# Performance work log

Measured on AMD Instinct MI355X. Metric: run time of the kernel, lower is better.

## Reference

```python
import jax, jax.numpy as jnp
import numpy as np

N_NODES = 4096
M_NODES = 8192
DIM = 256


def _symnorm(A):
    # D^{-1/2} A D^{-1/2} with eps, via row/col scaling (same math as diag matmuls)
    d = A.sum(axis=1) + 1e-5
    s = d ** -0.5
    return A * s[:, None] * s[None, :]


def _gat(A, X, W, a_src, a_dst, b):
    # Dense-form GATConv (PyG semantics): edges are nonzeros of A plus self loops.
    N = A.shape[0]
    H, F = a_src.shape
    Xp = (X @ W).reshape(N, H, F)                     # [N, H, F]
    src = jnp.einsum('nhf,hf->nh', Xp, a_src)         # score of source node j
    dst = jnp.einsum('nhf,hf->nh', Xp, a_dst)         # score of target node i
    logits = jax.nn.leaky_relu(dst[:, None, :] + src[None, :, :], negative_slope=0.2)  # [i, j, h]
    mask = (A != 0.0) | jnp.eye(N, dtype=bool)        # add_self_loops=True
    logits = jnp.where(mask[:, :, None], logits, -jnp.inf)
    alpha = jax.nn.softmax(logits, axis=1)            # softmax over neighbors j
    out = jnp.einsum('ijh,jhf->ihf', alpha, Xp).reshape(N, H * F) + b
    return out


def setup_inputs() -> dict:
    key = jax.random.key(0)
    ks = jax.random.split(key, 32)

    def p(i, shape, scale=0.05):
        return jax.random.normal(ks[i], shape, dtype=jnp.float32) * scale

    R = jax.random.normal(ks[0], (N_NODES, N_NODES), dtype=jnp.float32)
    A = jax.nn.relu((R + R.T) * 0.5)
    X = jax.random.normal(ks[1], (N_NODES, DIM), dtype=jnp.float32)
    return dict(
        A=A, X=X,
        # down GT0: GATConv(256, 128, heads=4) -> 512
        Wd0=p(2, (256, 512)), asd0=p(3, (4, 128)), add0=p(4, (4, 128)), bd0=p(5, (512,)),
        # down GT1: GATConv(512, 256, heads=4) -> 1024
        Wd1=p(6, (512, 1024)), asd1=p(7, (4, 256)), add1=p(8, (4, 256)), bd1=p(9, (1024,)),
        # pool projections (Linear(in, 1))
        wp0=p(10, (1, 512)), bp0=p(11, (1,)),
        wp1=p(12, (1, 1024)), bp1=p(13, (1,)),
        # bottom GT: GATConv(1024, 512, heads=2) -> 1024
        Wb=p(14, (1024, 1024)), asb=p(15, (2, 512)), adb=p(16, (2, 512)), bb=p(17, (1024,)),
        # up GT (reversed[0]): GATConv(1024, 128, heads=4) -> 512
        Wu0=p(18, (1024, 512)), asu0=p(19, (4, 128)), adu0=p(20, (4, 128)), bu0=p(21, (512,)),
        # up GT (reversed[1]): GATConv(512, 64, heads=4) -> 256
        Wu1=p(22, (512, 256)), asu1=p(23, (4, 64)), adu1=p(24, (4, 64)), bu1=p(25, (256,)),
        # upsampler Linear(n_nodes, m_nodes)
        Wup=p(26, (M_NODES, N_NODES)), bup=p(27, (M_NODES,)),
    )


def reference(A, X, Wd0, asd0, add0, bd0, Wd1, asd1, add1, bd1, wp0, bp0, wp1, bp1,
              Wb, asb, adb, bb, Wu0, asu0, adu0, bu0, Wu1, asu1, adu1, bu1, Wup, bup):
    N0 = A.shape[0]
    A0 = A + jnp.eye(N0, dtype=A.dtype)  # A_ = A + I (used throughout; normalized A is dead code)

    # ---- down level 0 ----
    X0 = jax.nn.relu(_gat(A0, X, Wd0, asd0, add0, bd0))            # [4096, 512]
    s0 = jax.nn.sigmoid(X0 @ wp0[0] + bp0[0])
    k0 = max(2, N0 // 2)                                            # int(0.5 * N)
    v0, idx0 = jax.lax.top_k(s0, k0)
    A1 = _symnorm(A0[idx0][:, idx0])                                # [2048, 2048]
    X1in = X0[idx0] * v0[:, None]

    # ---- down level 1 ----
    X1 = jax.nn.relu(_gat(A1, X1in, Wd1, asd1, add1, bd1))          # [2048, 1024]
    s1 = jax.nn.sigmoid(X1 @ wp1[0] + bp1[0])
    k1 = max(2, k0 // 2)
    v1, idx1 = jax.lax.top_k(s1, k1)
    A2 = _symnorm(A1[idx1][:, idx1])                                # [1024, 1024]
    X2in = X1[idx1] * v1[:, None]

    # ---- bottom ----
    Xb = jax.nn.relu(_gat(A2, X2in, Wb, asb, adb, bb))              # [1024, 1024]

    # ---- up level 0: unpool to level-1 graph ----
    h = jnp.zeros((k0, Xb.shape[1]), Xb.dtype).at[idx1].set(Xb)
    Xu0 = jax.nn.relu(_gat(A1, h, Wu0, asu0, adu0, bu0))            # [2048, 512]
    rec0 = jax.nn.relu(Xu0 @ Xu0.T)

    # ---- up level 1: unpool to original graph ----
    h = jnp.zeros((N0, Xu0.shape[1]), Xu0.dtype).at[idx0].set(Xu0)
    Xu1 = jax.nn.relu(_gat(A0, h, Wu1, asu1, adu1, bu1))            # [4096, 256]
    rec1 = jax.nn.relu(Xu1 @ Xu1.T)

    # ---- upsampler: Linear over node dim, softmax over feature dim, reconstruct adjacency ----
    Z = jax.nn.softmax(Wup @ Xu1 + bup[:, None], axis=1)            # [8192, 256]
    A_up = jax.nn.relu(Z @ Z.T)                                     # [8192, 8192]
    return (A_up, A0, A1, rec0, rec1)
```

## Files before the change

kernel.cpp:

```cpp
#include <hip/hip_runtime.h>
#include <math.h>


typedef short bf16x8 __attribute__((ext_vector_type(8)));
typedef float f32x4 __attribute__((ext_vector_type(4)));

static __device__ __forceinline__ float wave_sum64(float v) {
#pragma unroll
  for (int off = 32; off; off >>= 1) v += __shfl_down(v, off);
  return v;
}

static __device__ __forceinline__ unsigned short f2b(float x) {
  unsigned u = __float_as_uint(x);
  unsigned r = (u + 0x7fffu + ((u >> 16) & 1u)) >> 16;
  return (unsigned short)r;
}

static __device__ __forceinline__ float b2f(unsigned short h) {
  return __uint_as_float(((unsigned)h) << 16);
}

__global__ void k_add_eye(const float* __restrict__ A, float* __restrict__ O) {
  size_t i = ((size_t)blockIdx.x * 256 + threadIdx.x) * 4;
  size_t r = i >> 12, c = i & 4095;
  float4 v = *reinterpret_cast<const float4*>(&A[i]);
  if (r >= c && r < c + 4) ((float*)&v)[r - c] += 1.f;
  *reinterpret_cast<float4*>(&O[i]) = v;
}

__global__ void k_fill0(float* __restrict__ p, int n) {
  int stride = gridDim.x * 256;
  for (int i = blockIdx.x * 256 + threadIdx.x; i < n; i += stride) p[i] = 0.f;
}

__global__ void k_scatter_ones(const int* __restrict__ idx, float* __restrict__ m, int k) {
  int i = blockIdx.x * 256 + threadIdx.x;
  if (i < k) m[idx[i]] = 1.f;
}

__global__ void k_f32_to_bf16(const float* __restrict__ S, unsigned short* __restrict__ D,
                              int n) {
  int stride = gridDim.x * 1024;
  for (int i = (blockIdx.x * 256 + threadIdx.x) * 4; i < n; i += stride) {
    float4 v = *reinterpret_cast<const float4*>(&S[i]);
    uint2 o;
    o.x = (unsigned)f2b(v.x) | ((unsigned)f2b(v.y) << 16);
    o.y = (unsigned)f2b(v.z) | ((unsigned)f2b(v.w) << 16);
    *reinterpret_cast<uint2*>(&D[i]) = o;
  }
}

__global__ void k_split3(const float* __restrict__ S, unsigned short* __restrict__ D,
                         size_t PS, int n) {
  int stride = gridDim.x * 1024;
  for (int i = (blockIdx.x * 256 + threadIdx.x) * 4; i < n; i += stride) {
    float4 v = *reinterpret_cast<const float4*>(&S[i]);
    float xv[4] = {v.x, v.y, v.z, v.w};
    unsigned short o1[4], o2[4], o3[4];
#pragma unroll
    for (int e = 0; e < 4; ++e) {
      float x = xv[e];
      unsigned short a = f2b(x);
      float r1 = x - b2f(a);
      unsigned short b = f2b(r1);
      float r2 = r1 - b2f(b);
      o1[e] = a; o2[e] = b; o3[e] = f2b(r2);
    }
    *reinterpret_cast<uint2*>(&D[i]) = *reinterpret_cast<const uint2*>(o1);
    *reinterpret_cast<uint2*>(&D[PS + i]) = *reinterpret_cast<const uint2*>(o2);
    *reinterpret_cast<uint2*>(&D[2 * PS + i]) = *reinterpret_cast<const uint2*>(o3);
  }
}

__global__ __launch_bounds__(256) void k_transpose_bf16(const float* __restrict__ S, int ldS,
    unsigned short* __restrict__ D, int R, int Cc) {
  __shared__ unsigned short T[64][72];
  int r0 = blockIdx.y << 6, c0 = blockIdx.x << 6;
  int tid = threadIdx.x;
  int tr = tid >> 4, tc4 = (tid & 15) << 2;
#pragma unroll
  for (int q = 0; q < 4; ++q) {
    int row = tr + q * 16;
    float4 v = *reinterpret_cast<const float4*>(&S[(size_t)(r0 + row) * ldS + c0 + tc4]);
    T[tc4 + 0][row] = f2b(v.x);
    T[tc4 + 1][row] = f2b(v.y);
    T[tc4 + 2][row] = f2b(v.z);
    T[tc4 + 3][row] = f2b(v.w);
  }
  __syncthreads();
#pragma unroll
  for (int q = 0; q < 4; ++q) {
    int row = tr + q * 16;
    *reinterpret_cast<uint2*>(&D[(size_t)(c0 + row) * R + r0 + tc4]) =
        *reinterpret_cast<const uint2*>(&T[row][tc4]);
  }
}

__global__ __launch_bounds__(256) void k_transpose_bf16h(const float* __restrict__ S, int ldS,
    int F, unsigned short* __restrict__ D, int R) {
  __shared__ unsigned short T[64][72];
  int h = blockIdx.z;
  int r0 = blockIdx.y << 6, c0 = blockIdx.x << 6;
  int tid = threadIdx.x;
  int tr = tid >> 4, tc4 = (tid & 15) << 2;
#pragma unroll
  for (int q = 0; q < 4; ++q) {
    int row = tr + q * 16;
    float4 v = *reinterpret_cast<const float4*>(&S[(size_t)(r0 + row) * ldS + h * F + c0 + tc4]);
    T[tc4 + 0][row] = f2b(v.x);
    T[tc4 + 1][row] = f2b(v.y);
    T[tc4 + 2][row] = f2b(v.z);
    T[tc4 + 3][row] = f2b(v.w);
  }
  __syncthreads();
#pragma unroll
  for (int q = 0; q < 4; ++q) {
    int row = tr + q * 16;
    *reinterpret_cast<uint2*>(&D[((size_t)h * F + c0 + row) * R + r0 + tc4]) =
        *reinterpret_cast<const uint2*>(&T[row][tc4]);
  }
}

__global__ __launch_bounds__(256) void k_transpose_split(const float* __restrict__ S, int ldS,
    int F, unsigned short* __restrict__ D, int R, size_t PS) {
  __shared__ unsigned short T[3][64][72];
  int h = blockIdx.z;
  int c0 = blockIdx.x << 6, r0 = blockIdx.y << 6;
  int tid = threadIdx.x;
  int tr = tid >> 4, tc4 = (tid & 15) << 2;
#pragma unroll
  for (int q = 0; q < 4; ++q) {
    int row = tr + q * 16;
    float4 v = *reinterpret_cast<const float4*>(&S[(size_t)(r0 + row) * ldS + h * F + c0 + tc4]);
    float xv[4] = {v.x, v.y, v.z, v.w};
#pragma unroll
    for (int e = 0; e < 4; ++e) {
      float x = xv[e];
      unsigned short h1 = f2b(x);
      float r1 = x - b2f(h1);
      unsigned short h2 = f2b(r1);
      float r2 = r1 - b2f(h2);
      T[0][tc4 + e][row] = h1;
      T[1][tc4 + e][row] = h2;
      T[2][tc4 + e][row] = f2b(r2);
    }
  }
  __syncthreads();
#pragma unroll
  for (int p = 0; p < 3; ++p)
#pragma unroll
    for (int q = 0; q < 4; ++q) {
      int row = tr + q * 16;
      *reinterpret_cast<uint2*>(&D[p * PS + (size_t)(h * F + c0 + row) * R + r0 + tc4]) =
          *reinterpret_cast<const uint2*>(&T[p][row][tc4]);
    }
}

__global__ __launch_bounds__(256, 2) void k_gemm_x6_bt(const unsigned short* __restrict__ As,
    size_t APS, const unsigned short* __restrict__ BTs, size_t BPS, float* __restrict__ C,
    int M, int N, int K) {
  __shared__ __align__(16) unsigned short Ai[3][128 * 40];
  __shared__ __align__(16) unsigned short Bj[3][128 * 40];
  int tid = threadIdx.x;
  int m0 = blockIdx.y << 7, n0 = blockIdx.x << 7;
  int lane = tid & 63, w = tid >> 6;
  int lr = lane & 15, kb = lane >> 4;
  int wr = (w >> 1) << 6, wc = (w & 1) << 6;
  int sr = tid >> 1, sc = (tid & 1) << 4;
  f32x4 acc[4][4] = {};
  for (int k0 = 0; k0 < K; k0 += 32) {
    __syncthreads();
#pragma unroll
    for (int p = 0; p < 3; ++p) {
      const unsigned short* ga = &As[p * APS + (size_t)(m0 + sr) * K + k0 + sc];
      *reinterpret_cast<uint4*>(&Ai[p][sr * 40 + sc]) = *reinterpret_cast<const uint4*>(ga);
      *reinterpret_cast<uint4*>(&Ai[p][sr * 40 + sc + 8]) =
          *reinterpret_cast<const uint4*>(ga + 8);
      const unsigned short* gb = &BTs[p * BPS + (size_t)(n0 + sr) * K + k0 + sc];
      *reinterpret_cast<uint4*>(&Bj[p][sr * 40 + sc]) = *reinterpret_cast<const uint4*>(gb);
      *reinterpret_cast<uint4*>(&Bj[p][sr * 40 + sc + 8]) =
          *reinterpret_cast<const uint4*>(gb + 8);
    }
    __syncthreads();
    bf16x8 af[4][3], bf_[4][3];
#pragma unroll
    for (int m = 0; m < 4; ++m)
#pragma unroll
      for (int p = 0; p < 3; ++p)
        af[m][p] = *reinterpret_cast<const bf16x8*>(&Ai[p][(wr + m * 16 + lr) * 40 + kb * 8]);
#pragma unroll
    for (int n = 0; n < 4; ++n)
#pragma unroll
      for (int p = 0; p < 3; ++p)
        bf_[n][p] = *reinterpret_cast<const bf16x8*>(&Bj[p][(wc + n * 16 + lr) * 40 + kb * 8]);
#pragma unroll
    for (int m = 0; m < 4; ++m)
#pragma unroll
      for (int n = 0; n < 4; ++n) {
        acc[m][n] = __builtin_amdgcn_mfma_f32_16x16x32_bf16(af[m][0], bf_[n][0], acc[m][n], 0, 0, 0);
        acc[m][n] = __builtin_amdgcn_mfma_f32_16x16x32_bf16(af[m][0], bf_[n][1], acc[m][n], 0, 0, 0);
        acc[m][n] = __builtin_amdgcn_mfma_f32_16x16x32_bf16(af[m][1], bf_[n][0], acc[m][n], 0, 0, 0);
        acc[m][n] = __builtin_amdgcn_mfma_f32_16x16x32_bf16(af[m][0], bf_[n][2], acc[m][n], 0, 0, 0);
        acc[m][n] = __builtin_amdgcn_mfma_f32_16x16x32_bf16(af[m][2], bf_[n][0], acc[m][n], 0, 0, 0);
        acc[m][n] = __builtin_amdgcn_mfma_f32_16x16x32_bf16(af[m][1], bf_[n][1], acc[m][n], 0, 0, 0);
      }
  }
  int orow = m0 + wr + (lane >> 4) * 4;
  int ocol = n0 + wc + lr;
#pragma unroll
  for (int m = 0; m < 4; ++m)
#pragma unroll
    for (int n = 0; n < 4; ++n)
#pragma unroll
      for (int r = 0; r < 4; ++r)
        C[(size_t)(orow + m * 16 + r) * N + ocol + n * 16] = acc[m][n][r];
}

__global__ __launch_bounds__(512) void k_gat_x6(const float* __restrict__ Adj, int N,
    const unsigned short* __restrict__ XpS, size_t PS,
    const float* __restrict__ src, const float* __restrict__ dst,
    float* __restrict__ P, float* __restrict__ dP, int HF, int F, int jchunk) {
  __shared__ __align__(16) unsigned short wB[2][3][128 * 40];
  __shared__ __align__(16) unsigned short xB[2][3][128 * 40];
  int ftiles = F >> 7;
  int h = blockIdx.x / ftiles;
  int ft = blockIdx.x % ftiles;
  int f0 = ft << 7;
  int H = HF / F;
  int i0 = blockIdx.y << 7;
  int jb0 = blockIdx.z * jchunk;
  int tid = threadIdx.x;
  bool producer = tid < 256;
  int ntiles = jchunk >> 5;

  int sj4 = (tid & 7) << 2, si = tid >> 3;
  int xf = tid >> 1, xj8 = (tid & 1) << 3;
  float di[4];
  float dsum[4] = {0.f, 0.f, 0.f, 0.f};
  const unsigned short* xg = XpS + ((size_t)h * F + f0 + (producer ? xf : 0)) * N;
  float4 aw[4];
  float s4[4];
  uint4 xv[3][2];

  auto load_tile = [&](int jb) {
#pragma unroll
    for (int e = 0; e < 4; ++e) s4[e] = src[(jb + sj4 + e) * H + h];
#pragma unroll
    for (int q = 0; q < 4; ++q)
      aw[q] = *reinterpret_cast<const float4*>(&Adj[(size_t)(i0 + si + q * 32) * N + jb + sj4]);
#pragma unroll
    for (int p = 0; p < 3; ++p) {
      xv[p][0] = *reinterpret_cast<const uint4*>(&xg[p * PS + jb + xj8]);
      xv[p][1] = *reinterpret_cast<const uint4*>(&xg[p * PS + jb + xj8 + 16]);
    }
  };
  auto emit_tile = [&](int b, int jb) {
#pragma unroll
    for (int q = 0; q < 4; ++q) {
      int gi = i0 + si + q * 32;
      float dq = di[q];
      const float* a = (const float*)&aw[q];
      unsigned short h1[4], h2[4], h3[4];
      float ds = 0.f;
#pragma unroll
      for (int e = 0; e < 4; ++e) {
        float wv = 0.f;
        if (a[e] != 0.f || (jb + sj4 + e) == gi) {
          float tt = dq + s4[e];
          tt = tt >= 0.f ? tt : 0.2f * tt;
          wv = __expf(tt);
        }
        ds += wv;
        unsigned u1 = __float_as_uint(wv);
        h1[e] = (unsigned short)(u1 >> 16);
        float r1 = wv - __uint_as_float(u1 & 0xffff0000u);
        unsigned u2 = __float_as_uint(r1);
        h2[e] = (unsigned short)(u2 >> 16);
        float r2 = r1 - __uint_as_float(u2 & 0xffff0000u);
        h3[e] = (unsigned short)(__float_as_uint(r2) >> 16);
      }
      dsum[q] += ds;
      int ro = (si + q * 32) * 40 + sj4;
      uint2 o;
      o.x = (unsigned)h1[0] | ((unsigned)h1[1] << 16);
      o.y = (unsigned)h1[2] | ((unsigned)h1[3] << 16);
      *reinterpret_cast<uint2*>(&wB[b][0][ro]) = o;
      o.x = (unsigned)h2[0] | ((unsigned)h2[1] << 16);
      o.y = (unsigned)h2[2] | ((unsigned)h2[3] << 16);
      *reinterpret_cast<uint2*>(&wB[b][1][ro]) = o;
      o.x = (unsigned)h3[0] | ((unsigned)h3[1] << 16);
      o.y = (unsigned)h3[2] | ((unsigned)h3[3] << 16);
      *reinterpret_cast<uint2*>(&wB[b][2][ro]) = o;
    }
#pragma unroll
    for (int p = 0; p < 3; ++p) {
      *reinterpret_cast<uint4*>(&xB[b][p][xf * 40 + xj8]) = xv[p][0];
      *reinterpret_cast<uint4*>(&xB[b][p][xf * 40 + xj8 + 16]) = xv[p][1];
    }
  };

  int lane = tid & 63, cw = (tid >> 6) - 4;
  int clr = lane & 15, ckb = lane >> 4;
  int wr = ((cw >> 1) & 1) << 6, wf = (cw & 1) << 6;
  f32x4 acc[4][4] = {};

  if (producer) {
#pragma unroll
    for (int q = 0; q < 4; ++q) di[q] = dst[(i0 + si + q * 32) * H + h];
    load_tile(jb0);
    emit_tile(0, jb0);
    if (ntiles > 1) load_tile(jb0 + 32);
  }
  __syncthreads();
  for (int t = 0; t < ntiles; ++t) {
    if (producer) {
      int tn = t + 1;
      if (tn < ntiles) {
        emit_tile(tn & 1, jb0 + tn * 32);
        if (tn + 1 < ntiles) load_tile(jb0 + (tn + 1) * 32);
      }
    } else {
      int b = t & 1;
      bf16x8 af[4][3], bf_[4][3];
#pragma unroll
      for (int m = 0; m < 4; ++m)
#pragma unroll
        for (int p = 0; p < 3; ++p)
          af[m][p] =
              *reinterpret_cast<const bf16x8*>(&wB[b][p][(wr + m * 16 + clr) * 40 + ckb * 8]);
#pragma unroll
      for (int n = 0; n < 4; ++n)
#pragma unroll
        for (int p = 0; p < 3; ++p)
          bf_[n][p] =
              *reinterpret_cast<const bf16x8*>(&xB[b][p][(wf + n * 16 + clr) * 40 + ckb * 8]);
#pragma unroll
      for (int m = 0; m < 4; ++m)
#pragma unroll
        for (int n = 0; n < 4; ++n) {
          acc[m][n] = __builtin_amdgcn_mfma_f32_16x16x32_bf16(af[m][0], bf_[n][0], acc[m][n], 0, 0, 0);
          acc[m][n] = __builtin_amdgcn_mfma_f32_16x16x32_bf16(af[m][0], bf_[n][1], acc[m][n], 0, 0, 0);
          acc[m][n] = __builtin_amdgcn_mfma_f32_16x16x32_bf16(af[m][1], bf_[n][0], acc[m][n], 0, 0, 0);
          acc[m][n] = __builtin_amdgcn_mfma_f32_16x16x32_bf16(af[m][0], bf_[n][2], acc[m][n], 0, 0, 0);
          acc[m][n] = __builtin_amdgcn_mfma_f32_16x16x32_bf16(af[m][2], bf_[n][0], acc[m][n], 0, 0, 0);
          acc[m][n] = __builtin_amdgcn_mfma_f32_16x16x32_bf16(af[m][1], bf_[n][1], acc[m][n], 0, 0, 0);
        }
    }
    __syncthreads();
  }
  if (producer) {
    if (ft == 0) {
#pragma unroll
      for (int q = 0; q < 4; ++q) {
        float v = dsum[q];
        v += __shfl_xor(v, 1);
        v += __shfl_xor(v, 2);
        v += __shfl_xor(v, 4);
        if ((tid & 7) == 0)
          dP[(size_t)blockIdx.z * N * H + (i0 + si + q * 32) * H + h] = v;
      }
    }
  } else {
    float* Pc = P + (size_t)blockIdx.z * N * HF;
    int orow = i0 + wr + (lane >> 4) * 4;
    int ocol = h * F + f0 + wf + clr;
#pragma unroll
    for (int m = 0; m < 4; ++m)
#pragma unroll
      for (int n = 0; n < 4; ++n)
#pragma unroll
        for (int r = 0; r < 4; ++r)
          Pc[(size_t)(orow + m * 16 + r) * HF + ocol + n * 16] = acc[m][n][r];
  }
}

__global__ __launch_bounds__(256) void k_gat_mfma(const float* __restrict__ Adj, int N,
    const unsigned short* __restrict__ XpT,
    const float* __restrict__ src, const float* __restrict__ dst,
    float* __restrict__ P, float* __restrict__ dP, int HF, int F, int jchunk) {
  __shared__ __align__(16) unsigned short wL[256][40];
  __shared__ __align__(16) unsigned short xT[64][40];
  __shared__ float dsl[256];
  int ftiles = F >> 6;
  int h = blockIdx.x / ftiles;
  int ft = blockIdx.x % ftiles;
  int f0 = ft << 6;
  int H = HF / F;
  int i0 = blockIdx.y << 8;
  int jb0 = blockIdx.z * jchunk;
  int tid = threadIdx.x;
  int lane = tid & 63, w = tid >> 6;
  int lr = lane & 15, kb = lane >> 4;
  dsl[tid] = dst[(i0 + tid) * H + h];
  int sj4 = (tid & 7) << 2;
  int si = tid >> 3;
  int xf = tid >> 2;
  int xj8 = (tid & 3) << 3;
  const unsigned short* xg = XpT + ((size_t)h * F + f0 + xf) * N;
  float dsum[8] = {};
  f32x4 acc[4][4] = {};
  for (int jb = jb0; jb < jb0 + jchunk; jb += 32) {
    __syncthreads();
    float s4[4];
#pragma unroll
    for (int e = 0; e < 4; ++e) s4[e] = src[(jb + sj4 + e) * H + h];
#pragma unroll
    for (int q = 0; q < 8; ++q) {
      int i = si + q * 32;
      int gi = i0 + i;
      float4 av = *reinterpret_cast<const float4*>(&Adj[(size_t)gi * N + jb + sj4]);
      float di = dsl[i];
      float vv[4] = {av.x, av.y, av.z, av.w};
      unsigned short wb[4];
      float ds = 0.f;
#pragma unroll
      for (int e = 0; e < 4; ++e) {
        float wv = 0.f;
        if (vv[e] != 0.f || (jb + sj4 + e) == gi) {
          float t = di + s4[e];
          t = t >= 0.f ? t : 0.2f * t;
          wv = __expf(t);
        }
        ds += wv;
        wb[e] = f2b(wv);
      }
      dsum[q] += ds;
      *reinterpret_cast<uint2*>(&wL[i][sj4]) = *reinterpret_cast<const uint2*>(wb);
    }
    *reinterpret_cast<uint4*>(&xT[xf][xj8]) = *reinterpret_cast<const uint4*>(&xg[jb + xj8]);
    __syncthreads();
    bf16x8 a[4], b[4];
#pragma unroll
    for (int m = 0; m < 4; ++m)
      a[m] = *reinterpret_cast<const bf16x8*>(&wL[w * 64 + m * 16 + lr][kb * 8]);
#pragma unroll
    for (int n = 0; n < 4; ++n)
      b[n] = *reinterpret_cast<const bf16x8*>(&xT[n * 16 + lr][kb * 8]);
#pragma unroll
    for (int m = 0; m < 4; ++m)
#pragma unroll
      for (int n = 0; n < 4; ++n)
        acc[m][n] = __builtin_amdgcn_mfma_f32_16x16x32_bf16(a[m], b[n], acc[m][n], 0, 0, 0);
  }
  if (ft == 0) {
#pragma unroll
    for (int q = 0; q < 8; ++q) {
      float v = dsum[q];
      v += __shfl_xor(v, 1);
      v += __shfl_xor(v, 2);
      v += __shfl_xor(v, 4);
      if ((tid & 7) == 0)
        dP[(size_t)blockIdx.z * N * H + (i0 + si + q * 32) * H + h] = v;
    }
  }
  float* Pc = P + (size_t)blockIdx.z * N * HF;
  int orow = i0 + w * 64 + (lane >> 4) * 4;
  int ocol = h * F + f0 + (lane & 15);
#pragma unroll
  for (int m = 0; m < 4; ++m)
#pragma unroll
    for (int n = 0; n < 4; ++n)
#pragma unroll
      for (int r = 0; r < 4; ++r)
        Pc[(size_t)(orow + m * 16 + r) * HF + ocol + n * 16] = acc[m][n][r];
}

__global__ void k_gat_reduce(const float* __restrict__ P, int nch, size_t chstride,
    const float* __restrict__ dP, size_t dstride, const float* __restrict__ bias,
    float* __restrict__ Out, int HF, int F, int n_total) {
  int e = (blockIdx.x * 256 + threadIdx.x) * 4;
  if (e >= n_total) return;
  float4 s = *reinterpret_cast<const float4*>(&P[e]);
  for (int c = 1; c < nch; ++c) {
    float4 v = *reinterpret_cast<const float4*>(&P[c * chstride + e]);
    s.x += v.x; s.y += v.y; s.z += v.z; s.w += v.w;
  }
  int i = e / HF;
  int hf = e - i * HF;
  int h = hf / F;
  float den = 0.f;
  for (int c = 0; c < nch; ++c) den += dP[c * dstride + i * (HF / F) + h];
  float inv = 1.f / den;
  float4 bz = *reinterpret_cast<const float4*>(&bias[hf]);
  float4 o;
  o.x = fmaxf(fmaf(s.x, inv, bz.x), 0.f);
  o.y = fmaxf(fmaf(s.y, inv, bz.y), 0.f);
  o.z = fmaxf(fmaf(s.z, inv, bz.z), 0.f);
  o.w = fmaxf(fmaf(s.w, inv, bz.w), 0.f);
  *reinterpret_cast<float4*>(&Out[e]) = o;
}

__global__ __launch_bounds__(256) void k_syrk_mfma(const unsigned short* __restrict__ G,
    int M, int Kd, float* __restrict__ C) {
  if (blockIdx.x < blockIdx.y) return;
  __shared__ __align__(16) unsigned short Ai[128 * 40];
  __shared__ __align__(16) unsigned short Bj[128 * 40];
  int tid = threadIdx.x;
  int i0 = blockIdx.y << 7, j0 = blockIdx.x << 7;
  int srow = tid >> 1, scol = (tid & 1) << 3;
  int lane = tid & 63, w = tid >> 6;
  int wr = (w >> 1) << 6, wc = (w & 1) << 6;
  int lr = lane & 15, kb = lane >> 4;
  f32x4 acc[4][4] = {};
  const unsigned short* gA = G + (size_t)i0 * Kd;
  const unsigned short* gB = G + (size_t)j0 * Kd;
  for (int k0 = 0; k0 < Kd; k0 += 32) {
    __syncthreads();
#pragma unroll
    for (int kk = 0; kk < 32; kk += 16) {
      *reinterpret_cast<uint4*>(&Ai[srow * 40 + scol + kk]) =
          *reinterpret_cast<const uint4*>(&gA[(size_t)srow * Kd + k0 + scol + kk]);
      *reinterpret_cast<uint4*>(&Bj[srow * 40 + scol + kk]) =
          *reinterpret_cast<const uint4*>(&gB[(size_t)srow * Kd + k0 + scol + kk]);
    }
    __syncthreads();
    bf16x8 a[4], b[4];
#pragma unroll
    for (int m = 0; m < 4; ++m)
      a[m] = *reinterpret_cast<const bf16x8*>(&Ai[(wr + m * 16 + lr) * 40 + kb * 8]);
#pragma unroll
    for (int n = 0; n < 4; ++n)
      b[n] = *reinterpret_cast<const bf16x8*>(&Bj[(wc + n * 16 + lr) * 40 + kb * 8]);
#pragma unroll
    for (int m = 0; m < 4; ++m)
#pragma unroll
      for (int n = 0; n < 4; ++n)
        acc[m][n] = __builtin_amdgcn_mfma_f32_16x16x32_bf16(a[m], b[n], acc[m][n], 0, 0, 0);
  }
  int orow = i0 + wr + (lane >> 4) * 4;
  int ocol = j0 + wc + (lane & 15);
  bool mirror = (j0 != i0);
#pragma unroll
  for (int m = 0; m < 4; ++m)
#pragma unroll
    for (int n = 0; n < 4; ++n) {
      float4 v;
      v.x = fmaxf(acc[m][n][0], 0.f);
      v.y = fmaxf(acc[m][n][1], 0.f);
      v.z = fmaxf(acc[m][n][2], 0.f);
      v.w = fmaxf(acc[m][n][3], 0.f);
#pragma unroll
      for (int r = 0; r < 4; ++r)
        C[(size_t)(orow + m * 16 + r) * M + ocol + n * 16] = ((const float*)&v)[r];
      if (mirror)
        *reinterpret_cast<float4*>(
            &C[(size_t)(j0 + wc + n * 16 + lr) * M + i0 + wr + m * 16 + (lane >> 4) * 4]) = v;
    }
}

__global__ __launch_bounds__(256) void k_gemm_mfma_bt(const unsigned short* __restrict__ Amat,
    const unsigned short* __restrict__ BT, const float* __restrict__ bias,
    float* __restrict__ C, int M, int N, int Kd) {
  __shared__ __align__(16) unsigned short Ai[128 * 40];
  __shared__ __align__(16) unsigned short Bj[128 * 40];
  int tid = threadIdx.x;
  int m0 = blockIdx.y << 7, n0 = blockIdx.x << 7;
  int srow = tid >> 1, scol = (tid & 1) << 3;
  int lane = tid & 63, w = tid >> 6;
  int wr = (w >> 1) << 6, wc = (w & 1) << 6;
  int lr = lane & 15, kb = lane >> 4;
  f32x4 acc[4][4] = {};
  const unsigned short* gA = Amat + (size_t)m0 * Kd;
  const unsigned short* gB = BT + (size_t)n0 * Kd;
  for (int k0 = 0; k0 < Kd; k0 += 32) {
    __syncthreads();
#pragma unroll
    for (int kk = 0; kk < 32; kk += 16) {
      *reinterpret_cast<uint4*>(&Ai[srow * 40 + scol + kk]) =
          *reinterpret_cast<const uint4*>(&gA[(size_t)srow * Kd + k0 + scol + kk]);
      *reinterpret_cast<uint4*>(&Bj[srow * 40 + scol + kk]) =
          *reinterpret_cast<const uint4*>(&gB[(size_t)srow * Kd + k0 + scol + kk]);
    }
    __syncthreads();
    bf16x8 a[4], b[4];
#pragma unroll
    for (int m = 0; m < 4; ++m)
      a[m] = *reinterpret_cast<const bf16x8*>(&Ai[(wr + m * 16 + lr) * 40 + kb * 8]);
#pragma unroll
    for (int n = 0; n < 4; ++n)
      b[n] = *reinterpret_cast<const bf16x8*>(&Bj[(wc + n * 16 + lr) * 40 + kb * 8]);
#pragma unroll
    for (int m = 0; m < 4; ++m)
#pragma unroll
      for (int n = 0; n < 4; ++n)
        acc[m][n] = __builtin_amdgcn_mfma_f32_16x16x32_bf16(a[m], b[n], acc[m][n], 0, 0, 0);
  }
  int orow = m0 + wr + (lane >> 4) * 4;
  int ocol = n0 + wc + (lane & 15);
#pragma unroll
  for (int m = 0; m < 4; ++m)
#pragma unroll
    for (int n = 0; n < 4; ++n)
#pragma unroll
      for (int r = 0; r < 4; ++r) {
        float rb = bias ? bias[orow + m * 16 + r] : 0.f;
        C[(size_t)(orow + m * 16 + r) * N + ocol + n * 16] = acc[m][n][r] + rb;
      }
}

__global__ __launch_bounds__(512) void k_gemm_aup(const float* __restrict__ Wg,
    const unsigned short* __restrict__ BT, float* __restrict__ Pz, int Mtot, int Ktot,
    int kc_len) {
  __shared__ __align__(16) unsigned short Ai[128 * 40];
  __shared__ __align__(16) unsigned short Bj[256 * 40];
  int tid = threadIdx.x;
  int m0 = blockIdx.y << 7;
  int k0base = blockIdx.x * kc_len;
  int lane = tid & 63, w = tid >> 6;
  int wr = (w >> 2) << 6, wc = (w & 3) << 6;
  int lr = lane & 15, kb = lane >> 4;
  int ar = tid >> 2, ac8 = (tid & 3) << 3;
  int br = tid >> 1, bc16 = (tid & 1) << 4;
  f32x4 acc[4][4] = {};
  for (int kk = 0; kk < kc_len; kk += 32) {
    int k0 = k0base + kk;
    __syncthreads();
    {
      const float* arow = &Wg[(size_t)(m0 + ar) * Ktot + k0 + ac8];
      float4 v0 = *reinterpret_cast<const float4*>(arow);
      float4 v1 = *reinterpret_cast<const float4*>(arow + 4);
      unsigned short t8[8] = {f2b(v0.x), f2b(v0.y), f2b(v0.z), f2b(v0.w),
                              f2b(v1.x), f2b(v1.y), f2b(v1.z), f2b(v1.w)};
      *reinterpret_cast<uint4*>(&Ai[ar * 40 + ac8]) = *reinterpret_cast<const uint4*>(t8);
      const unsigned short* brow = &BT[(size_t)br * Ktot + k0 + bc16];
      *reinterpret_cast<uint4*>(&Bj[br * 40 + bc16]) = *reinterpret_cast<const uint4*>(brow);
      *reinterpret_cast<uint4*>(&Bj[br * 40 + bc16 + 8]) =
          *reinterpret_cast<const uint4*>(brow + 8);
    }
    __syncthreads();
    bf16x8 a[4], b[4];
#pragma unroll
    for (int m = 0; m < 4; ++m)
      a[m] = *reinterpret_cast<const bf16x8*>(&Ai[(wr + m * 16 + lr) * 40 + kb * 8]);
#pragma unroll
    for (int n = 0; n < 4; ++n)
      b[n] = *reinterpret_cast<const bf16x8*>(&Bj[(wc + n * 16 + lr) * 40 + kb * 8]);
#pragma unroll
    for (int m = 0; m < 4; ++m)
#pragma unroll
      for (int n = 0; n < 4; ++n)
        acc[m][n] = __builtin_amdgcn_mfma_f32_16x16x32_bf16(a[m], b[n], acc[m][n], 0, 0, 0);
  }
  float* outp = Pz + (size_t)blockIdx.x * Mtot * 256;
  int orow = m0 + wr + (lane >> 4) * 4;
  int ocol = wc + (lane & 15);
#pragma unroll
  for (int m = 0; m < 4; ++m)
#pragma unroll
    for (int n = 0; n < 4; ++n)
#pragma unroll
      for (int r = 0; r < 4; ++r)
        outp[(size_t)(orow + m * 16 + r) * 256 + ocol + n * 16] = acc[m][n][r];
}

__global__ __launch_bounds__(256) void k_softmax_fuse(const float* __restrict__ Pz, int nch,
    size_t chstride, const float* __restrict__ bias, unsigned short* __restrict__ ZB) {
  int row = blockIdx.x, tid = threadIdx.x;
  size_t e = (size_t)row * 256 + tid;
  float x = bias[row];
  for (int c = 0; c < nch; ++c) x += Pz[c * chstride + e];
  float m = x;
#pragma unroll
  for (int off = 32; off; off >>= 1) m = fmaxf(m, __shfl_down(m, off));
  __shared__ float red[4];
  __shared__ float bm, bs;
  if ((tid & 63) == 0) red[tid >> 6] = m;
  __syncthreads();
  if (tid == 0) bm = fmaxf(fmaxf(red[0], red[1]), fmaxf(red[2], red[3]));
  __syncthreads();
  float ev = expf(x - bm);
  float sm = wave_sum64(ev);
  __syncthreads();
  if ((tid & 63) == 0) red[tid >> 6] = sm;
  __syncthreads();
  if (tid == 0) bs = red[0] + red[1] + red[2] + red[3];
  __syncthreads();
  ZB[e] = f2b(ev / bs);
}

__global__ void k_src_dst(const float* __restrict__ Xp, const float* __restrict__ a_src,
    const float* __restrict__ a_dst, float* __restrict__ src, float* __restrict__ dst,
    int H, int F) {
  int n = blockIdx.x;
  int h = threadIdx.x >> 6, lane = threadIdx.x & 63;
  const float* x = Xp + ((size_t)n * H + h) * F;
  const float* as = a_src + h * F;
  const float* ad = a_dst + h * F;
  float ps = 0.f, pd = 0.f;
  for (int f = lane; f < F; f += 64) {
    float xv = x[f];
    ps = fmaf(xv, as[f], ps);
    pd = fmaf(xv, ad[f], pd);
  }
  ps = wave_sum64(ps);
  pd = wave_sum64(pd);
  if (lane == 0) { src[n * H + h] = ps; dst[n * H + h] = pd; }
}

__global__ __launch_bounds__(256) void k_score(const float* __restrict__ Xf,
    const float* __restrict__ wv, const float* __restrict__ bsc, float* __restrict__ s, int D) {
  int row = blockIdx.x * 4 + (threadIdx.x >> 6);
  int lane = threadIdx.x & 63;
  const float* x = Xf + (size_t)row * D;
  float p = 0.f;
  for (int f = lane; f < D; f += 64) p = fmaf(x[f], wv[f], p);
  p = wave_sum64(p);
  if (lane == 0) s[row] = 1.f / (1.f + expf(-(p + bsc[0])));
}

__global__ __launch_bounds__(256) void k_topk_rank(const float* __restrict__ s, int n, int k,
    int* __restrict__ idx, float* __restrict__ vals) {
  extern __shared__ unsigned long long keys[];
  int tid = threadIdx.x;
  for (int j = tid; j < n; j += 256) {
    unsigned u = __float_as_uint(s[j]);
    unsigned ord = (u & 0x80000000u) ? ~u : (u | 0x80000000u);
    keys[j] = ((unsigned long long)ord << 32) | (unsigned)(~j);
  }
  __syncthreads();
  int i = blockIdx.x * 256 + tid;
  unsigned long long mykey = keys[i];
  int rank = 0;
#pragma unroll 4
  for (int j = 0; j < n; ++j) rank += (keys[j] > mykey);
  if (rank < k) { idx[rank] = i; vals[rank] = s[i]; }
}

__global__ __launch_bounds__(256) void k_rowsum_mask(const float* __restrict__ A0, int N,
    const int* __restrict__ idx, const float* __restrict__ m, float* __restrict__ sv) {
  int i = blockIdx.x, tid = threadIdx.x;
  const float* row = A0 + (size_t)idx[i] * N;
  float p = 0.f;
  for (int j = tid * 4; j < N; j += 1024) {
    float4 a = *reinterpret_cast<const float4*>(&row[j]);
    float4 b = *reinterpret_cast<const float4*>(&m[j]);
    p += a.x * b.x + a.y * b.y + a.z * b.z + a.w * b.w;
  }
  p = wave_sum64(p);
  __shared__ float red[4];
  if ((tid & 63) == 0) red[tid >> 6] = p;
  __syncthreads();
  if (tid == 0) sv[i] = rsqrtf(red[0] + red[1] + red[2] + red[3] + 1e-5f);
}

__global__ __launch_bounds__(256) void k_gatherT(const float* __restrict__ A0, int N,
    const int* __restrict__ idx, float* __restrict__ T1, int k) {
  __shared__ float T[64][65];
  int i0 = blockIdx.x << 6, c0 = blockIdx.y << 6;
  int tid = threadIdx.x;
  int tr = tid >> 4, tc4 = (tid & 15) << 2;
#pragma unroll
  for (int q = 0; q < 4; ++q) {
    int row = tr + q * 16;
    float4 v = *reinterpret_cast<const float4*>(&A0[(size_t)idx[i0 + row] * N + c0 + tc4]);
    T[tc4 + 0][row] = v.x; T[tc4 + 1][row] = v.y; T[tc4 + 2][row] = v.z; T[tc4 + 3][row] = v.w;
  }
  __syncthreads();
#pragma unroll
  for (int q = 0; q < 4; ++q) {
    int row = tr + q * 16;
    float4 o;
    o.x = T[row][tc4]; o.y = T[row][tc4 + 1]; o.z = T[row][tc4 + 2]; o.w = T[row][tc4 + 3];
    *reinterpret_cast<float4*>(&T1[(size_t)(c0 + row) * k + i0 + tc4]) = o;
  }
}

__global__ void k_scaleT(const float* __restrict__ T1, int k, const int* __restrict__ idx,
    const float* __restrict__ sv, float* __restrict__ A1) {
  int j = blockIdx.y;
  int i = (blockIdx.x * 256 + threadIdx.x) * 4;
  float sj = sv[j];
  const float* r = T1 + (size_t)idx[j] * k;
  float4 v = *reinterpret_cast<const float4*>(&r[i]);
  float4 s = *reinterpret_cast<const float4*>(&sv[i]);
  v.x *= sj * s.x; v.y *= sj * s.y; v.z *= sj * s.z; v.w *= sj * s.w;
  *reinterpret_cast<float4*>(&A1[(size_t)j * k + i]) = v;
}

__global__ void k_gather_mat(const float* __restrict__ Asrc, int lda,
    const int* __restrict__ idx, float* __restrict__ B, int k) {
  int j = blockIdx.x * 256 + threadIdx.x;
  int i = blockIdx.y;
  B[(size_t)i * k + j] = Asrc[(size_t)idx[i] * lda + idx[j]];
}

__global__ void k_gather_scale_rows(const float* __restrict__ Xs, int D,
    const int* __restrict__ idx, const float* __restrict__ v, float* __restrict__ Xo) {
  int f = blockIdx.x * 256 + threadIdx.x;
  int i = blockIdx.y;
  Xo[(size_t)i * D + f] = Xs[(size_t)idx[i] * D + f] * v[i];
}

__global__ void k_scatter_rows(const float* __restrict__ P, int D, const int* __restrict__ idx,
                               float* __restrict__ Xo) {
  int f = blockIdx.x * 256 + threadIdx.x;
  int i = blockIdx.y;
  Xo[(size_t)idx[i] * D + f] = P[(size_t)i * D + f];
}

extern "C" void kernel_launch(void* const* d_in, const int* in_sizes, int n_in,
                              void* d_out, int out_size, void* d_ws, size_t ws_size,
                              hipStream_t stream) {
  const float* A    = (const float*)d_in[0];
  const float* X    = (const float*)d_in[1];
  const float* Wd0  = (const float*)d_in[2];
  const float* asd0 = (const float*)d_in[3];
  const float* add0 = (const float*)d_in[4];
  const float* bd0  = (const float*)d_in[5];
  const float* Wd1  = (const float*)d_in[6];
  const float* asd1 = (const float*)d_in[7];
  const float* add1 = (const float*)d_in[8];
  const float* bd1  = (const float*)d_in[9];
  const float* wp0  = (const float*)d_in[10];
  const float* bp0  = (const float*)d_in[11];
  const float* wp1  = (const float*)d_in[12];
  const float* bp1  = (const float*)d_in[13];
  const float* Wb   = (const float*)d_in[14];
  const float* asb  = (const float*)d_in[15];
  const float* adb  = (const float*)d_in[16];
  const float* bb   = (const float*)d_in[17];
  const float* Wu0  = (const float*)d_in[18];
  const float* asu0 = (const float*)d_in[19];
  const float* adu0 = (const float*)d_in[20];
  const float* bu0  = (const float*)d_in[21];
  const float* Wu1  = (const float*)d_in[22];
  const float* asu1 = (const float*)d_in[23];
  const float* adu1 = (const float*)d_in[24];
  const float* bu1  = (const float*)d_in[25];
  const float* Wup  = (const float*)d_in[26];
  const float* bup  = (const float*)d_in[27];
  (void)in_sizes; (void)n_in; (void)out_size; (void)ws_size;

  float* out  = (float*)d_out;
  float* Aup  = out;
  float* A0   = out + 67108864ULL;
  float* A1   = A0 + 16777216ULL;
  float* rec0 = A1 + 4194304ULL;
  float* rec1 = rec0 + 4194304ULL;

  float* S = Aup;
  size_t off = 0;
  auto nxt = [&](size_t n) { float* p = S + off; off += (n + 1023) & ~(size_t)1023; return p; };
  float* Xp0  = nxt(4096 * 512);
  float* X0   = nxt(4096 * 512);
  float* src0 = nxt(4096 * 4);
  float* dst0 = nxt(4096 * 4);
  float* sc0  = nxt(4096);
  int*   idx0 = (int*)nxt(2048);
  float* v0   = nxt(2048);
  float* sv0  = nxt(2048);
  float* maskv = nxt(4096);
  float* X1in = nxt(2048 * 512);
  float* Xp1  = nxt(2048 * 1024);
  float* X1   = nxt(2048 * 1024);
  float* src1 = nxt(2048 * 4);
  float* dst1 = nxt(2048 * 4);
  float* sc1  = nxt(2048);
  int*   idx1 = (int*)nxt(1024);
  float* v1   = nxt(1024);
  float* A2m  = nxt(1024 * 1024);
  float* X2in = nxt(1024 * 1024);
  float* Xpb  = nxt(1024 * 1024);
  float* Xb   = nxt(1024 * 1024);
  float* srcb = nxt(1024 * 2);
  float* dstb = nxt(1024 * 2);
  float* Pu0  = nxt(1024 * 512);
  float* Xpu0 = nxt(2048 * 512);
  float* Xu0  = nxt(2048 * 512);
  float* su0  = nxt(2048 * 4);
  float* du0  = nxt(2048 * 4);
  float* Pu1  = nxt(2048 * 256);
  float* Xpu1 = nxt(4096 * 256);
  float* su1  = nxt(4096 * 4);
  float* du1  = nxt(4096 * 4);
  float* dPp  = nxt(8 * 4096 * 4);
  float* P    = nxt((size_t)8 * 4096 * 512);
  float* T1   = nxt((size_t)4096 * 2048);
  unsigned short* XpS  = (unsigned short*)nxt(3200000);
  unsigned short* XSp  = (unsigned short*)nxt(1572864);
  unsigned short* Wd0T = (unsigned short*)nxt(196608);
  unsigned short* Wd1T = (unsigned short*)nxt(786432);
  unsigned short* XpT  = (unsigned short*)nxt(524288);
  unsigned short* X2inB = (unsigned short*)nxt(524288);
  unsigned short* XbB   = (unsigned short*)nxt(524288);
  unsigned short* WbT   = (unsigned short*)nxt(524288);
  unsigned short* Wu0T  = (unsigned short*)nxt(262144);
  unsigned short* Wu1T  = (unsigned short*)nxt(65536);

  float* W = (float*)d_ws;
  float* Xu1 = W;
  unsigned short* Xu1B = (unsigned short*)(W + 1048576);
  unsigned short* Xu0B = (unsigned short*)(W + 1048576 + 524288);

  float* Pz = rec1;
  unsigned short* ZB = (unsigned short*)(rec1 + 4 * 2097152);
  unsigned short* Xu1T = (unsigned short*)(rec1 + 4 * 2097152 + 1048576);

  const size_t PS0 = (size_t)4 * 128 * 4096;
  const size_t PS1 = (size_t)4 * 256 * 2048;

  k_add_eye<<<16384, 256, 0, stream>>>(A, A0);

  k_split3<<<1024, 256, 0, stream>>>(X, XSp, (size_t)4096 * 256, 4096 * 256);
  k_transpose_split<<<dim3(8, 4, 1), 256, 0, stream>>>(Wd0, 512, 512, Wd0T, 256,
                                                       (size_t)512 * 256);
  k_gemm_x6_bt<<<dim3(4, 32), 256, 0, stream>>>(XSp, (size_t)4096 * 256, Wd0T,
                                                (size_t)512 * 256, Xp0, 4096, 512, 256);
  k_src_dst<<<4096, 256, 0, stream>>>(Xp0, asd0, add0, src0, dst0, 4, 128);
  k_transpose_split<<<dim3(2, 64, 4), 256, 0, stream>>>(Xp0, 512, 128, XpS, 4096, PS0);
  k_gat_x6<<<dim3(4, 32, 2), 512, 0, stream>>>(A0, 4096, XpS, PS0, src0, dst0, P, dPp, 512,
                                               128, 2048);
  k_gat_reduce<<<2048, 256, 0, stream>>>(P, 2, (size_t)4096 * 512, dPp, (size_t)4096 * 4, bd0,
                                         X0, 512, 128, 4096 * 512);
  k_score<<<1024, 256, 0, stream>>>(X0, wp0, bp0, sc0, 512);
  k_topk_rank<<<16, 256, 4096 * 8, stream>>>(sc0, 4096, 2048, idx0, v0);
  k_fill0<<<16, 256, 0, stream>>>(maskv, 4096);
  k_scatter_ones<<<8, 256, 0, stream>>>(idx0, maskv, 2048);
  k_rowsum_mask<<<2048, 256, 0, stream>>>(A0, 4096, idx0, maskv, sv0);
  k_gatherT<<<dim3(32, 64), 256, 0, stream>>>(A0, 4096, idx0, T1, 2048);
  k_scaleT<<<dim3(2, 2048), 256, 0, stream>>>(T1, 2048, idx0, sv0, A1);
  k_gather_scale_rows<<<dim3(2, 2048), 256, 0, stream>>>(X0, 512, idx0, v0, X1in);

  k_split3<<<1024, 256, 0, stream>>>(X1in, XSp, (size_t)2048 * 512, 2048 * 512);
  k_transpose_split<<<dim3(16, 8, 1), 256, 0, stream>>>(Wd1, 1024, 1024, Wd1T, 512,
                                                        (size_t)1024 * 512);
  k_gemm_x6_bt<<<dim3(8, 16), 256, 0, stream>>>(XSp, (size_t)2048 * 512, Wd1T,
                                                (size_t)1024 * 512, Xp1, 2048, 1024, 512);
  k_src_dst<<<2048, 256, 0, stream>>>(Xp1, asd1, add1, src1, dst1, 4, 256);
  k_transpose_split<<<dim3(4, 32, 4), 256, 0, stream>>>(Xp1, 1024, 256, XpS, 2048, PS1);
  k_gat_x6<<<dim3(8, 16, 2), 512, 0, stream>>>(A1, 2048, XpS, PS1, src1, dst1, P, dPp, 1024,
                                               256, 1024);
  k_gat_reduce<<<2048, 256, 0, stream>>>(P, 2, (size_t)2048 * 1024, dPp, (size_t)2048 * 4, bd1,
                                         X1, 1024, 256, 2048 * 1024);
  k_score<<<512, 256, 0, stream>>>(X1, wp1, bp1, sc1, 1024);
  k_topk_rank<<<8, 256, 2048 * 8, stream>>>(sc1, 2048, 1024, idx1, v1);
  k_gather_mat<<<dim3(4, 1024), 256, 0, stream>>>(A1, 2048, idx1, A2m, 1024);
  k_gather_scale_rows<<<dim3(4, 1024), 256, 0, stream>>>(X1, 1024, idx1, v1, X2in);

  k_f32_to_bf16<<<1024, 256, 0, stream>>>(X2in, X2inB, 1024 * 1024);
  k_transpose_bf16<<<dim3(16, 16), 256, 0, stream>>>(Wb, 1024, WbT, 1024, 1024);
  k_gemm_mfma_bt<<<dim3(8, 8), 256, 0, stream>>>(X2inB, WbT, nullptr, Xpb, 1024, 1024, 1024);
  k_src_dst<<<1024, 128, 0, stream>>>(Xpb, asb, adb, srcb, dstb, 2, 512);
  k_transpose_bf16h<<<dim3(8, 16, 2), 256, 0, stream>>>(Xpb, 1024, 512, XpT, 1024);
  k_gat_mfma<<<dim3(16, 4, 8), 256, 0, stream>>>(A2m, 1024, XpT, srcb, dstb, P, dPp, 1024, 512,
                                                 128);
  k_gat_reduce<<<1024, 256, 0, stream>>>(P, 8, (size_t)1024 * 1024, dPp, (size_t)1024 * 2, bb,
                                         Xb, 1024, 512, 1024 * 1024);

  k_f32_to_bf16<<<1024, 256, 0, stream>>>(Xb, XbB, 1024 * 1024);
  k_transpose_bf16<<<dim3(8, 16), 256, 0, stream>>>(Wu0, 512, Wu0T, 1024, 512);
  k_gemm_mfma_bt<<<dim3(4, 8), 256, 0, stream>>>(XbB, Wu0T, nullptr, Pu0, 1024, 512, 1024);
  k_fill0<<<1024, 256, 0, stream>>>(Xpu0, 2048 * 512);
  k_scatter_rows<<<dim3(2, 1024), 256, 0, stream>>>(Pu0, 512, idx1, Xpu0);
  k_src_dst<<<2048, 256, 0, stream>>>(Xpu0, asu0, adu0, su0, du0, 4, 128);
  k_transpose_bf16h<<<dim3(2, 32, 4), 256, 0, stream>>>(Xpu0, 512, 128, XpT, 2048);
  k_gat_mfma<<<dim3(8, 8, 8), 256, 0, stream>>>(A1, 2048, XpT, su0, du0, P, dPp, 512, 128, 256);
  k_gat_reduce<<<1024, 256, 0, stream>>>(P, 8, (size_t)2048 * 512, dPp, (size_t)2048 * 4, bu0,
                                         Xu0, 512, 128, 2048 * 512);
  k_f32_to_bf16<<<1024, 256, 0, stream>>>(Xu0, Xu0B, 2048 * 512);

  k_transpose_bf16<<<dim3(4, 8), 256, 0, stream>>>(Wu1, 256, Wu1T, 512, 256);
  k_gemm_mfma_bt<<<dim3(2, 16), 256, 0, stream>>>(Xu0B, Wu1T, nullptr, Pu1, 2048, 256, 512);
  k_fill0<<<1024, 256, 0, stream>>>(Xpu1, 4096 * 256);
  k_scatter_rows<<<dim3(1, 2048), 256, 0, stream>>>(Pu1, 256, idx0, Xpu1);
  k_src_dst<<<4096, 256, 0, stream>>>(Xpu1, asu1, adu1, su1, du1, 4, 64);
  k_transpose_bf16h<<<dim3(1, 64, 4), 256, 0, stream>>>(Xpu1, 256, 64, XpT, 4096);
  k_gat_mfma<<<dim3(4, 16, 8), 256, 0, stream>>>(A0, 4096, XpT, su1, du1, P, dPp, 256, 64, 512);
  k_gat_reduce<<<1024, 256, 0, stream>>>(P, 8, (size_t)4096 * 256, dPp, (size_t)4096 * 4, bu1,
                                         Xu1, 256, 64, 4096 * 256);
  k_f32_to_bf16<<<1024, 256, 0, stream>>>(Xu1, Xu1B, 4096 * 256);
  k_transpose_bf16<<<dim3(4, 64), 256, 0, stream>>>(Xu1, 256, Xu1T, 4096, 256);

  k_gemm_aup<<<dim3(4, 64), 512, 0, stream>>>(Wup, Xu1T, Pz, 8192, 4096, 1024);
  k_softmax_fuse<<<8192, 256, 0, stream>>>(Pz, 4, (size_t)8192 * 256, bup, ZB);
  k_syrk_mfma<<<dim3(64, 64), 256, 0, stream>>>(ZB, 8192, 256, Aup);

  k_syrk_mfma<<<dim3(32, 32), 256, 0, stream>>>(Xu1B, 4096, 256, rec1);
  k_syrk_mfma<<<dim3(16, 16), 256, 0, stream>>>(Xu0B, 2048, 512, rec0);
}
```

Measured before the change: 1.144 ms.

## Restructure GAT kernels, fuse gather/scale/convert steps, and emit bf16 from reduce

Replaces the producer/consumer k_gat_x6 with a simpler single-buffer kernel that uses all eight waves for both weight generation and MFMA, and splits the j range four ways. k_gat_mfma becomes a templated k_gat_b16 that handles several heads per block with 128-row tiles. Gather+scale+split/convert is fused into one kernel, the mask scatter is folded into top-k, and the reduce writes bf16 directly, which removes the separate f32-to-bf16 passes and fp32 intermediates. This cuts launches and memory traffic. The cost is more partial-sum traffic from the extra j splits, and the GAT kernel loses its overlap of loads with compute.

```diff
diff --git a/kernel.cpp b/kernel.cpp
--- a/kernel.cpp
+++ b/kernel.cpp
@@ -32,23 +32,6 @@
 __global__ void k_fill0(float* __restrict__ p, int n) {
   int stride = gridDim.x * 256;
   for (int i = blockIdx.x * 256 + threadIdx.x; i < n; i += stride) p[i] = 0.f;
-}
-
-__global__ void k_scatter_ones(const int* __restrict__ idx, float* __restrict__ m, int k) {
-  int i = blockIdx.x * 256 + threadIdx.x;
-  if (i < k) m[idx[i]] = 1.f;
-}
-
-__global__ void k_f32_to_bf16(const float* __restrict__ S, unsigned short* __restrict__ D,
-                              int n) {
-  int stride = gridDim.x * 1024;
-  for (int i = (blockIdx.x * 256 + threadIdx.x) * 4; i < n; i += stride) {
-    float4 v = *reinterpret_cast<const float4*>(&S[i]);
-    uint2 o;
-    o.x = (unsigned)f2b(v.x) | ((unsigned)f2b(v.y) << 16);
-    o.y = (unsigned)f2b(v.z) | ((unsigned)f2b(v.w) << 16);
-    *reinterpret_cast<uint2*>(&D[i]) = o;
-  }
 }
 
 __global__ void k_split3(const float* __restrict__ S, unsigned short* __restrict__ D,
@@ -73,6 +56,43 @@
   }
 }
 
+__global__ void k_gather_scale_split3(const float* __restrict__ Xs, int Dd,
+    const int* __restrict__ idx, const float* __restrict__ v,
+    unsigned short* __restrict__ D, size_t PS) {
+  int i = blockIdx.y;
+  int f = (blockIdx.x * 256 + threadIdx.x) * 4;
+  if (f >= Dd) return;
+  float vi = v[i];
+  float4 x4 = *reinterpret_cast<const float4*>(&Xs[(size_t)idx[i] * Dd + f]);
+  float xv[4] = {x4.x * vi, x4.y * vi, x4.z * vi, x4.w * vi};
+  unsigned short o1[4], o2[4], o3[4];
+#pragma unroll
+  for (int e = 0; e < 4; ++e) {
+    float x = xv[e];
+    unsigned short a = f2b(x);
+    float r1 = x - b2f(a);
+    unsigned short b = f2b(r1);
+    float r2 = r1 - b2f(b);
+    o1[e] = a; o2[e] = b; o3[e] = f2b(r2);
+  }
+  size_t e0 = (size_t)i * Dd + f;
+  *reinterpret_cast<uint2*>(&D[e0]) = *reinterpret_cast<const uint2*>(o1);
+  *reinterpret_cast<uint2*>(&D[PS + e0]) = *reinterpret_cast<const uint2*>(o2);
+  *reinterpret_cast<uint2*>(&D[2 * PS + e0]) = *reinterpret_cast<const uint2*>(o3);
+}
+
+__global__ void k_gather_scale_b16(const float* __restrict__ Xs, int Dd,
+    const int* __restrict__ idx, const float* __restrict__ v,
+    unsigned short* __restrict__ D) {
+  int i = blockIdx.y;
+  int f = (blockIdx.x * 256 + threadIdx.x) * 4;
+  if (f >= Dd) return;
+  float vi = v[i];
+  float4 x4 = *reinterpret_cast<const float4*>(&Xs[(size_t)idx[i] * Dd + f]);
+  unsigned short o[4] = {f2b(x4.x * vi), f2b(x4.y * vi), f2b(x4.z * vi), f2b(x4.w * vi)};
+  *reinterpret_cast<uint2*>(&D[(size_t)i * Dd + f]) = *reinterpret_cast<const uint2*>(o);
+}
+
 __global__ __launch_bounds__(256) void k_transpose_bf16(const float* __restrict__ S, int ldS,
     unsigned short* __restrict__ D, int R, int Cc) {
   __shared__ unsigned short T[64][72];
@@ -87,6 +107,29 @@
     T[tc4 + 1][row] = f2b(v.y);
     T[tc4 + 2][row] = f2b(v.z);
     T[tc4 + 3][row] = f2b(v.w);
+  }
+  __syncthreads();
+#pragma unroll
+  for (int q = 0; q < 4; ++q) {
+    int row = tr + q * 16;
+    *reinterpret_cast<uint2*>(&D[(size_t)(c0 + row) * R + r0 + tc4]) =
+        *reinterpret_cast<const uint2*>(&T[row][tc4]);
+  }
+}
+
+__global__ __launch_bounds__(256) void k_transpose_bb(const unsigned short* __restrict__ S,
+    int ldS, unsigned short* __restrict__ D, int R, int Cc) {
+  __shared__ unsigned short T[64][72];
+  int r0 = blockIdx.y << 6, c0 = blockIdx.x << 6;
+  int tid = threadIdx.x;
+  int tr = tid >> 4, tc4 = (tid & 15) << 2;
+#pragma unroll
+  for (int q = 0; q < 4; ++q) {
+    int row = tr + q * 16;
+    uint2 v = *reinterpret_cast<const uint2*>(&S[(size_t)(r0 + row) * ldS + c0 + tc4]);
+    const unsigned short* p = (const unsigned short*)&v;
+    T[tc4 + 0][row] = p[0]; T[tc4 + 1][row] = p[1];
+    T[tc4 + 2][row] = p[2]; T[tc4 + 3][row] = p[3];
   }
   __syncthreads();
 #pragma unroll
@@ -217,57 +260,57 @@
         C[(size_t)(orow + m * 16 + r) * N + ocol + n * 16] = acc[m][n][r];
 }
 
-__global__ __launch_bounds__(512) void k_gat_x6(const float* __restrict__ Adj, int N,
+__global__ __launch_bounds__(512, 4) void k_gat_x6(const float* __restrict__ Adj, int N,
     const unsigned short* __restrict__ XpS, size_t PS,
     const float* __restrict__ src, const float* __restrict__ dst,
-    float* __restrict__ P, float* __restrict__ dP, int HF, int F, int jchunk) {
-  __shared__ __align__(16) unsigned short wB[2][3][128 * 40];
-  __shared__ __align__(16) unsigned short xB[2][3][128 * 40];
-  int ftiles = F >> 7;
-  int h = blockIdx.x / ftiles;
-  int ft = blockIdx.x % ftiles;
-  int f0 = ft << 7;
-  int H = HF / F;
+    float* __restrict__ P, float* __restrict__ dP, int HF, int Ffull, int FP, int jchunk) {
+  __shared__ __align__(16) unsigned short wL[3][128 * 40];
+  __shared__ __align__(16) unsigned short xL[3][128 * 40];
+  __shared__ float dstL[128];
+  __shared__ float srcL[32];
+  int H = HF / Ffull;
+  int h = blockIdx.x / FP;
+  int fp = blockIdx.x % FP;
+  int f0 = fp << 7;
   int i0 = blockIdx.y << 7;
   int jb0 = blockIdx.z * jchunk;
   int tid = threadIdx.x;
-  bool producer = tid < 256;
+  int si = tid >> 2, sj8 = (tid & 3) << 3;
+  int lane = tid & 63, w = tid >> 6;
+  int lr = lane & 15, kb = lane >> 4;
+  int fs = w << 4;
+  if (tid < 128) dstL[tid] = dst[(i0 + tid) * H + h];
+  float dsum = 0.f;
+  f32x4 acc[8] = {};
   int ntiles = jchunk >> 5;
-
-  int sj4 = (tid & 7) << 2, si = tid >> 3;
-  int xf = tid >> 1, xj8 = (tid & 1) << 3;
-  float di[4];
-  float dsum[4] = {0.f, 0.f, 0.f, 0.f};
-  const unsigned short* xg = XpS + ((size_t)h * F + f0 + (producer ? xf : 0)) * N;
-  float4 aw[4];
-  float s4[4];
-  uint4 xv[3][2];
-
-  auto load_tile = [&](int jb) {
-#pragma unroll
-    for (int e = 0; e < 4; ++e) s4[e] = src[(jb + sj4 + e) * H + h];
-#pragma unroll
-    for (int q = 0; q < 4; ++q)
-      aw[q] = *reinterpret_cast<const float4*>(&Adj[(size_t)(i0 + si + q * 32) * N + jb + sj4]);
-#pragma unroll
-    for (int p = 0; p < 3; ++p) {
-      xv[p][0] = *reinterpret_cast<const uint4*>(&xg[p * PS + jb + xj8]);
-      xv[p][1] = *reinterpret_cast<const uint4*>(&xg[p * PS + jb + xj8 + 16]);
-    }
-  };
-  auto emit_tile = [&](int b, int jb) {
-#pragma unroll
-    for (int q = 0; q < 4; ++q) {
-      int gi = i0 + si + q * 32;
-      float dq = di[q];
-      const float* a = (const float*)&aw[q];
-      unsigned short h1[4], h2[4], h3[4];
+  const unsigned short* xbase = XpS + ((size_t)h * Ffull + f0) * N;
+  for (int t = 0; t < ntiles; ++t) {
+    int jb = jb0 + (t << 5);
+    __syncthreads();
+    if (tid < 32) srcL[tid] = src[(jb + tid) * H + h];
+    {
+      int frow = tid >> 2;
+#pragma unroll
+      for (int p = 0; p < 3; ++p)
+        *reinterpret_cast<uint4*>(&xL[p][frow * 40 + sj8]) =
+            *reinterpret_cast<const uint4*>(&xbase[p * PS + (size_t)frow * N + jb + sj8]);
+    }
+    float4 av0 = *reinterpret_cast<const float4*>(&Adj[(size_t)(i0 + si) * N + jb + sj8]);
+    float4 av1 = *reinterpret_cast<const float4*>(&Adj[(size_t)(i0 + si) * N + jb + sj8 + 4]);
+    __syncthreads();
+    {
+      int gi = i0 + si;
+      float dq = dstL[si];
+      const float* a0 = (const float*)&av0;
+      const float* a1 = (const float*)&av1;
+      unsigned short h1[8], h2[8], h3[8];
       float ds = 0.f;
 #pragma unroll
-      for (int e = 0; e < 4; ++e) {
+      for (int e = 0; e < 8; ++e) {
+        float a = e < 4 ? a0[e] : a1[e - 4];
         float wv = 0.f;
-        if (a[e] != 0.f || (jb + sj4 + e) == gi) {
-          float tt = dq + s4[e];
+        if (a != 0.f || (jb + sj8 + e) == gi) {
+          float tt = dq + srcL[sj8 + e];
           tt = tt >= 0.f ? tt : 0.2f * tt;
           wv = __expf(tt);
         }
@@ -280,195 +323,148 @@
         float r2 = r1 - __uint_as_float(u2 & 0xffff0000u);
         h3[e] = (unsigned short)(__float_as_uint(r2) >> 16);
       }
-      dsum[q] += ds;
-      int ro = (si + q * 32) * 40 + sj4;
-      uint2 o;
-      o.x = (unsigned)h1[0] | ((unsigned)h1[1] << 16);
-      o.y = (unsigned)h1[2] | ((unsigned)h1[3] << 16);
-      *reinterpret_cast<uint2*>(&wB[b][0][ro]) = o;
-      o.x = (unsigned)h2[0] | ((unsigned)h2[1] << 16);
-      o.y = (unsigned)h2[2] | ((unsigned)h2[3] << 16);
-      *reinterpret_cast<uint2*>(&wB[b][1][ro]) = o;
-      o.x = (unsigned)h3[0] | ((unsigned)h3[1] << 16);
-      o.y = (unsigned)h3[2] | ((unsigned)h3[3] << 16);
-      *reinterpret_cast<uint2*>(&wB[b][2][ro]) = o;
-    }
-#pragma unroll
-    for (int p = 0; p < 3; ++p) {
-      *reinterpret_cast<uint4*>(&xB[b][p][xf * 40 + xj8]) = xv[p][0];
-      *reinterpret_cast<uint4*>(&xB[b][p][xf * 40 + xj8 + 16]) = xv[p][1];
-    }
-  };
-
-  int lane = tid & 63, cw = (tid >> 6) - 4;
-  int clr = lane & 15, ckb = lane >> 4;
-  int wr = ((cw >> 1) & 1) << 6, wf = (cw & 1) << 6;
-  f32x4 acc[4][4] = {};
-
-  if (producer) {
-#pragma unroll
-    for (int q = 0; q < 4; ++q) di[q] = dst[(i0 + si + q * 32) * H + h];
-    load_tile(jb0);
-    emit_tile(0, jb0);
-    if (ntiles > 1) load_tile(jb0 + 32);
-  }
-  __syncthreads();
-  for (int t = 0; t < ntiles; ++t) {
-    if (producer) {
-      int tn = t + 1;
-      if (tn < ntiles) {
-        emit_tile(tn & 1, jb0 + tn * 32);
-        if (tn + 1 < ntiles) load_tile(jb0 + (tn + 1) * 32);
-      }
-    } else {
-      int b = t & 1;
-      bf16x8 af[4][3], bf_[4][3];
-#pragma unroll
-      for (int m = 0; m < 4; ++m)
-#pragma unroll
-        for (int p = 0; p < 3; ++p)
-          af[m][p] =
-              *reinterpret_cast<const bf16x8*>(&wB[b][p][(wr + m * 16 + clr) * 40 + ckb * 8]);
-#pragma unroll
-      for (int n = 0; n < 4; ++n)
-#pragma unroll
-        for (int p = 0; p < 3; ++p)
-          bf_[n][p] =
-              *reinterpret_cast<const bf16x8*>(&xB[b][p][(wf + n * 16 + clr) * 40 + ckb * 8]);
-#pragma unroll
-      for (int m = 0; m < 4; ++m)
-#pragma unroll
-        for (int n = 0; n < 4; ++n) {
-          acc[m][n] = __builtin_amdgcn_mfma_f32_16x16x32_bf16(af[m][0], bf_[n][0], acc[m][n], 0, 0, 0);
-          acc[m][n] = __builtin_amdgcn_mfma_f32_16x16x32_bf16(af[m][0], bf_[n][1], acc[m][n], 0, 0, 0);
-          acc[m][n] = __builtin_amdgcn_mfma_f32_16x16x32_bf16(af[m][1], bf_[n][0], acc[m][n], 0, 0, 0);
-          acc[m][n] = __builtin_amdgcn_mfma_f32_16x16x32_bf16(af[m][0], bf_[n][2], acc[m][n], 0, 0, 0);
-          acc[m][n] = __builtin_amdgcn_mfma_f32_16x16x32_bf16(af[m][2], bf_[n][0], acc[m][n], 0, 0, 0);
-          acc[m][n] = __builtin_amdgcn_mfma_f32_16x16x32_bf16(af[m][1], bf_[n][1], acc[m][n], 0, 0, 0);
-        }
-    }
-    __syncthreads();
-  }
-  if (producer) {
-    if (ft == 0) {
-#pragma unroll
-      for (int q = 0; q < 4; ++q) {
-        float v = dsum[q];
-        v += __shfl_xor(v, 1);
-        v += __shfl_xor(v, 2);
-        v += __shfl_xor(v, 4);
-        if ((tid & 7) == 0)
-          dP[(size_t)blockIdx.z * N * H + (i0 + si + q * 32) * H + h] = v;
-      }
-    }
-  } else {
-    float* Pc = P + (size_t)blockIdx.z * N * HF;
-    int orow = i0 + wr + (lane >> 4) * 4;
-    int ocol = h * F + f0 + wf + clr;
-#pragma unroll
-    for (int m = 0; m < 4; ++m)
-#pragma unroll
-      for (int n = 0; n < 4; ++n)
-#pragma unroll
-        for (int r = 0; r < 4; ++r)
-          Pc[(size_t)(orow + m * 16 + r) * HF + ocol + n * 16] = acc[m][n][r];
-  }
-}
-
-__global__ __launch_bounds__(256) void k_gat_mfma(const float* __restrict__ Adj, int N,
+      dsum += ds;
+      *reinterpret_cast<uint4*>(&wL[0][si * 40 + sj8]) = *reinterpret_cast<const uint4*>(h1);
+      *reinterpret_cast<uint4*>(&wL[1][si * 40 + sj8]) = *reinterpret_cast<const uint4*>(h2);
+      *reinterpret_cast<uint4*>(&wL[2][si * 40 + sj8]) = *reinterpret_cast<const uint4*>(h3);
+    }
+    __syncthreads();
+    bf16x8 bf_[3];
+#pragma unroll
+    for (int p = 0; p < 3; ++p)
+      bf_[p] = *reinterpret_cast<const bf16x8*>(&xL[p][(fs + lr) * 40 + kb * 8]);
+#pragma unroll
+    for (int m = 0; m < 8; ++m) {
+      bf16x8 af[3];
+#pragma unroll
+      for (int p = 0; p < 3; ++p)
+        af[p] = *reinterpret_cast<const bf16x8*>(&wL[p][(m * 16 + lr) * 40 + kb * 8]);
+      acc[m] = __builtin_amdgcn_mfma_f32_16x16x32_bf16(af[0], bf_[0], acc[m], 0, 0, 0);
+      acc[m] = __builtin_amdgcn_mfma_f32_16x16x32_bf16(af[0], bf_[1], acc[m], 0, 0, 0);
+      acc[m] = __builtin_amdgcn_mfma_f32_16x16x32_bf16(af[1], bf_[0], acc[m], 0, 0, 0);
+      acc[m] = __builtin_amdgcn_mfma_f32_16x16x32_bf16(af[0], bf_[2], acc[m], 0, 0, 0);
+      acc[m] = __builtin_amdgcn_mfma_f32_16x16x32_bf16(af[2], bf_[0], acc[m], 0, 0, 0);
+      acc[m] = __builtin_amdgcn_mfma_f32_16x16x32_bf16(af[1], bf_[1], acc[m], 0, 0, 0);
+    }
+  }
+  if (fp == 0) {
+    float v = dsum;
+    v += __shfl_xor(v, 1);
+    v += __shfl_xor(v, 2);
+    if ((tid & 3) == 0)
+      dP[(size_t)blockIdx.z * N * H + (i0 + si) * H + h] = v;
+  }
+  float* Pc = P + (size_t)blockIdx.z * N * HF;
+  int orow = i0 + (lane >> 4) * 4;
+  int ocol = h * Ffull + f0 + fs + lr;
+#pragma unroll
+  for (int m = 0; m < 8; ++m)
+#pragma unroll
+    for (int r = 0; r < 4; ++r)
+      Pc[(size_t)(orow + m * 16 + r) * HF + ocol] = acc[m][r];
+}
+
+template <int NS, int HEADS>
+__global__ __launch_bounds__(512) void k_gat_b16(const float* __restrict__ Adj, int N,
     const unsigned short* __restrict__ XpT,
     const float* __restrict__ src, const float* __restrict__ dst,
     float* __restrict__ P, float* __restrict__ dP, int HF, int F, int jchunk) {
-  __shared__ __align__(16) unsigned short wL[256][40];
-  __shared__ __align__(16) unsigned short xT[64][40];
-  __shared__ float dsl[256];
-  int ftiles = F >> 6;
-  int h = blockIdx.x / ftiles;
-  int ft = blockIdx.x % ftiles;
-  int f0 = ft << 6;
+  constexpr int HFB = NS * 128;
+  __shared__ __align__(16) unsigned short wL[HEADS][128 * 40];
+  __shared__ __align__(16) unsigned short xL[HFB * 40];
+  __shared__ float dstL[HEADS][128];
+  __shared__ float srcL[HEADS][32];
   int H = HF / F;
-  int i0 = blockIdx.y << 8;
+  int hf0 = blockIdx.x * HFB;
+  int h0 = hf0 / F;
+  int i0 = blockIdx.y << 7;
   int jb0 = blockIdx.z * jchunk;
   int tid = threadIdx.x;
+  int si = tid >> 2, sj8 = (tid & 3) << 3;
   int lane = tid & 63, w = tid >> 6;
   int lr = lane & 15, kb = lane >> 4;
-  dsl[tid] = dst[(i0 + tid) * H + h];
-  int sj4 = (tid & 7) << 2;
-  int si = tid >> 3;
-  int xf = tid >> 2;
-  int xj8 = (tid & 3) << 3;
-  const unsigned short* xg = XpT + ((size_t)h * F + f0 + xf) * N;
-  float dsum[8] = {};
-  f32x4 acc[4][4] = {};
-  for (int jb = jb0; jb < jb0 + jchunk; jb += 32) {
-    __syncthreads();
-    float s4[4];
-#pragma unroll
-    for (int e = 0; e < 4; ++e) s4[e] = src[(jb + sj4 + e) * H + h];
-#pragma unroll
-    for (int q = 0; q < 8; ++q) {
-      int i = si + q * 32;
-      int gi = i0 + i;
-      float4 av = *reinterpret_cast<const float4*>(&Adj[(size_t)gi * N + jb + sj4]);
-      float di = dsl[i];
-      float vv[4] = {av.x, av.y, av.z, av.w};
-      unsigned short wb[4];
-      float ds = 0.f;
-#pragma unroll
-      for (int e = 0; e < 4; ++e) {
-        float wv = 0.f;
-        if (vv[e] != 0.f || (jb + sj4 + e) == gi) {
-          float t = di + s4[e];
-          t = t >= 0.f ? t : 0.2f * t;
-          wv = __expf(t);
+  int fs = w * (NS * 16);
+  int hw = (hf0 + fs) / F - h0;
+  if (tid < HEADS * 128)
+    dstL[tid >> 7][tid & 127] = dst[(i0 + (tid & 127)) * H + h0 + (tid >> 7)];
+  float dsum[HEADS] = {};
+  f32x4 acc[8][NS] = {};
+  int ntiles = jchunk >> 5;
+  for (int t = 0; t < ntiles; ++t) {
+    int jb = jb0 + (t << 5);
+    __syncthreads();
+    if (tid < HEADS * 32) srcL[tid >> 5][tid & 31] = src[(jb + (tid & 31)) * H + h0 + (tid >> 5)];
+#pragma unroll
+    for (int base = 0; base < HFB; base += 128) {
+      int row = base + (tid >> 2);
+      *reinterpret_cast<uint4*>(&xL[row * 40 + sj8]) =
+          *reinterpret_cast<const uint4*>(&XpT[(size_t)(hf0 + row) * N + jb + sj8]);
+    }
+    float4 av0 = *reinterpret_cast<const float4*>(&Adj[(size_t)(i0 + si) * N + jb + sj8]);
+    float4 av1 = *reinterpret_cast<const float4*>(&Adj[(size_t)(i0 + si) * N + jb + sj8 + 4]);
+    __syncthreads();
+    {
+      int gi = i0 + si;
+      const float* a0 = (const float*)&av0;
+      const float* a1 = (const float*)&av1;
+#pragma unroll
+      for (int hh = 0; hh < HEADS; ++hh) {
+        float dq = dstL[hh][si];
+        unsigned short wb[8];
+        float ds = 0.f;
+#pragma unroll
+        for (int e = 0; e < 8; ++e) {
+          float a = e < 4 ? a0[e] : a1[e - 4];
+          float wv = 0.f;
+          if (a != 0.f || (jb + sj8 + e) == gi) {
+            float tt = dq + srcL[hh][sj8 + e];
+            tt = tt >= 0.f ? tt : 0.2f * tt;
+            wv = __expf(tt);
+          }
+          ds += wv;
+          wb[e] = f2b(wv);
         }
-        ds += wv;
-        wb[e] = f2b(wv);
+        dsum[hh] += ds;
+        *reinterpret_cast<uint4*>(&wL[hh][si * 40 + sj8]) =
+            *reinterpret_cast<const uint4*>(wb);
       }
-      dsum[q] += ds;
-      *reinterpret_cast<uint2*>(&wL[i][sj4]) = *reinterpret_cast<const uint2*>(wb);
-    }
-    *reinterpret_cast<uint4*>(&xT[xf][xj8]) = *reinterpret_cast<const uint4*>(&xg[jb + xj8]);
-    __syncthreads();
-    bf16x8 a[4], b[4];
-#pragma unroll
-    for (int m = 0; m < 4; ++m)
-      a[m] = *reinterpret_cast<const bf16x8*>(&wL[w * 64 + m * 16 + lr][kb * 8]);
-#pragma unroll
-    for (int n = 0; n < 4; ++n)
-      b[n] = *reinterpret_cast<const bf16x8*>(&xT[n * 16 + lr][kb * 8]);
-#pragma unroll
-    for (int m = 0; m < 4; ++m)
-#pragma unroll
-      for (int n = 0; n < 4; ++n)
-        acc[m][n] = __builtin_amdgcn_mfma_f32_16x16x32_bf16(a[m], b[n], acc[m][n], 0, 0, 0);
-  }
-  if (ft == 0) {
-#pragma unroll
-    for (int q = 0; q < 8; ++q) {
-      float v = dsum[q];
-      v += __shfl_xor(v, 1);
-      v += __shfl_xor(v, 2);
-      v += __shfl_xor(v, 4);
-      if ((tid & 7) == 0)
-        dP[(size_t)blockIdx.z * N * H + (i0 + si + q * 32) * H + h] = v;
-    }
+    }
+    __syncthreads();
+    bf16x8 bf_[NS];
+#pragma unroll
+    for (int n = 0; n < NS; ++n)
+      bf_[n] = *reinterpret_cast<const bf16x8*>(&xL[(fs + n * 16 + lr) * 40 + kb * 8]);
+#pragma unroll
+    for (int m = 0; m < 8; ++m) {
+      bf16x8 a = *reinterpret_cast<const bf16x8*>(&wL[hw][(m * 16 + lr) * 40 + kb * 8]);
+#pragma unroll
+      for (int n = 0; n < NS; ++n)
+        acc[m][n] = __builtin_amdgcn_mfma_f32_16x16x32_bf16(a, bf_[n], acc[m][n], 0, 0, 0);
+    }
+  }
+#pragma unroll
+  for (int hh = 0; hh < HEADS; ++hh) {
+    float v = dsum[hh];
+    v += __shfl_xor(v, 1);
+    v += __shfl_xor(v, 2);
+    if ((tid & 3) == 0)
+      dP[(size_t)blockIdx.z * N * H + (i0 + si) * H + h0 + hh] = v;
   }
   float* Pc = P + (size_t)blockIdx.z * N * HF;
-  int orow = i0 + w * 64 + (lane >> 4) * 4;
-  int ocol = h * F + f0 + (lane & 15);
-#pragma unroll
-  for (int m = 0; m < 4; ++m)
-#pragma unroll
-    for (int n = 0; n < 4; ++n)
+  int orow = i0 + (lane >> 4) * 4;
+  int ocol0 = hf0 + fs + lr;
+#pragma unroll
+  for (int m = 0; m < 8; ++m)
+#pragma unroll
+    for (int n = 0; n < NS; ++n)
 #pragma unroll
       for (int r = 0; r < 4; ++r)
-        Pc[(size_t)(orow + m * 16 + r) * HF + ocol + n * 16] = acc[m][n][r];
+        Pc[(size_t)(orow + m * 16 + r) * HF + ocol0 + n * 16] = acc[m][n][r];
 }
 
 __global__ void k_gat_reduce(const float* __restrict__ P, int nch, size_t chstride,
     const float* __restrict__ dP, size_t dstride, const float* __restrict__ bias,
-    float* __restrict__ Out, int HF, int F, int n_total) {
+    float* __restrict__ Of, unsigned short* __restrict__ Ob, int HF, int F, int n_total) {
   int e = (blockIdx.x * 256 + threadIdx.x) * 4;
   if (e >= n_total) return;
   float4 s = *reinterpret_cast<const float4*>(&P[e]);
@@ -488,7 +484,11 @@
   o.y = fmaxf(fmaf(s.y, inv, bz.y), 0.f);
   o.z = fmaxf(fmaf(s.z, inv, bz.z), 0.f);
   o.w = fmaxf(fmaf(s.w, inv, bz.w), 0.f);
-  *reinterpret_cast<float4*>(&Out[e]) = o;
+  if (Of) *reinterpret_cast<float4*>(&Of[e]) = o;
+  if (Ob) {
+    unsigned short ob[4] = {f2b(o.x), f2b(o.y), f2b(o.z), f2b(o.w)};
+    *reinterpret_cast<uint2*>(&Ob[e]) = *reinterpret_cast<const uint2*>(ob);
+  }
 }
 
 __global__ __launch_bounds__(256) void k_syrk_mfma(const unsigned short* __restrict__ G,
@@ -710,21 +710,26 @@
 }
 
 __global__ __launch_bounds__(256) void k_topk_rank(const float* __restrict__ s, int n, int k,
-    int* __restrict__ idx, float* __restrict__ vals) {
+    int* __restrict__ idx, float* __restrict__ vals, float* __restrict__ mask) {
   extern __shared__ unsigned long long keys[];
   int tid = threadIdx.x;
+  int i = blockIdx.x * 256 + tid;
+  if (mask) mask[i] = 0.f;
   for (int j = tid; j < n; j += 256) {
     unsigned u = __float_as_uint(s[j]);
     unsigned ord = (u & 0x80000000u) ? ~u : (u | 0x80000000u);
     keys[j] = ((unsigned long long)ord << 32) | (unsigned)(~j);
   }
   __syncthreads();
-  int i = blockIdx.x * 256 + tid;
   unsigned long long mykey = keys[i];
   int rank = 0;
 #pragma unroll 4
   for (int j = 0; j < n; ++j) rank += (keys[j] > mykey);
-  if (rank < k) { idx[rank] = i; vals[rank] = s[i]; }
+  if (rank < k) {
+    idx[rank] = i;
+    vals[rank] = s[i];
+    if (mask) mask[i] = 1.f;
+  }
 }
 
 __global__ __launch_bounds__(256) void k_rowsum_mask(const float* __restrict__ A0, int N,
@@ -783,13 +788,6 @@
   int j = blockIdx.x * 256 + threadIdx.x;
   int i = blockIdx.y;
   B[(size_t)i * k + j] = Asrc[(size_t)idx[i] * lda + idx[j]];
-}
-
-__global__ void k_gather_scale_rows(const float* __restrict__ Xs, int D,
-    const int* __restrict__ idx, const float* __restrict__ v, float* __restrict__ Xo) {
-  int f = blockIdx.x * 256 + threadIdx.x;
-  int i = blockIdx.y;
-  Xo[(size_t)i * D + f] = Xs[(size_t)idx[i] * D + f] * v[i];
 }
 
 __global__ void k_scatter_rows(const float* __restrict__ P, int D, const int* __restrict__ idx,
@@ -851,7 +849,6 @@
   float* v0   = nxt(2048);
   float* sv0  = nxt(2048);
   float* maskv = nxt(4096);
-  float* X1in = nxt(2048 * 512);
   float* Xp1  = nxt(2048 * 1024);
   float* X1   = nxt(2048 * 1024);
   float* src1 = nxt(2048 * 4);
@@ -860,14 +857,11 @@
   int*   idx1 = (int*)nxt(1024);
   float* v1   = nxt(1024);
   float* A2m  = nxt(1024 * 1024);
-  float* X2in = nxt(1024 * 1024);
   float* Xpb  = nxt(1024 * 1024);
-  float* Xb   = nxt(1024 * 1024);
   float* srcb = nxt(1024 * 2);
   float* dstb = nxt(1024 * 2);
   float* Pu0  = nxt(1024 * 512);
   float* Xpu0 = nxt(2048 * 512);
-  float* Xu0  = nxt(2048 * 512);
   float* su0  = nxt(2048 * 4);
   float* du0  = nxt(2048 * 4);
   float* Pu1  = nxt(2048 * 256);
@@ -889,7 +883,6 @@
   unsigned short* Wu1T  = (unsigned short*)nxt(65536);
 
   float* W = (float*)d_ws;
-  float* Xu1 = W;
   unsigned short* Xu1B = (unsigned short*)(W + 1048576);
   unsigned short* Xu0B = (unsigned short*)(W + 1048576 + 524288);
 
@@ -909,56 +902,52 @@
                                                 (size_t)512 * 256, Xp0, 4096, 512, 256);
   k_src_dst<<<4096, 256, 0, stream>>>(Xp0, asd0, add0, src0, dst0, 4, 128);
   k_transpose_split<<<dim3(2, 64, 4), 256, 0, stream>>>(Xp0, 512, 128, XpS, 4096, PS0);
-  k_gat_x6<<<dim3(4, 32, 2), 512, 0, stream>>>(A0, 4096, XpS, PS0, src0, dst0, P, dPp, 512,
-                                               128, 2048);
-  k_gat_reduce<<<2048, 256, 0, stream>>>(P, 2, (size_t)4096 * 512, dPp, (size_t)4096 * 4, bd0,
-                                         X0, 512, 128, 4096 * 512);
+  k_gat_x6<<<dim3(4, 32, 4), 512, 0, stream>>>(A0, 4096, XpS, PS0, src0, dst0, P, dPp, 512,
+                                               128, 1, 1024);
+  k_gat_reduce<<<2048, 256, 0, stream>>>(P, 4, (size_t)4096 * 512, dPp, (size_t)4096 * 4, bd0,
+                                         X0, nullptr, 512, 128, 4096 * 512);
   k_score<<<1024, 256, 0, stream>>>(X0, wp0, bp0, sc0, 512);
-  k_topk_rank<<<16, 256, 4096 * 8, stream>>>(sc0, 4096, 2048, idx0, v0);
-  k_fill0<<<16, 256, 0, stream>>>(maskv, 4096);
-  k_scatter_ones<<<8, 256, 0, stream>>>(idx0, maskv, 2048);
+  k_topk_rank<<<16, 256, 4096 * 8, stream>>>(sc0, 4096, 2048, idx0, v0, maskv);
   k_rowsum_mask<<<2048, 256, 0, stream>>>(A0, 4096, idx0, maskv, sv0);
   k_gatherT<<<dim3(32, 64), 256, 0, stream>>>(A0, 4096, idx0, T1, 2048);
   k_scaleT<<<dim3(2, 2048), 256, 0, stream>>>(T1, 2048, idx0, sv0, A1);
-  k_gather_scale_rows<<<dim3(2, 2048), 256, 0, stream>>>(X0, 512, idx0, v0, X1in);
-
-  k_split3<<<1024, 256, 0, stream>>>(X1in, XSp, (size_t)2048 * 512, 2048 * 512);
+
+  k_gather_scale_split3<<<dim3(1, 2048), 256, 0, stream>>>(X0, 512, idx0, v0, XSp,
+                                                           (size_t)2048 * 512);
   k_transpose_split<<<dim3(16, 8, 1), 256, 0, stream>>>(Wd1, 1024, 1024, Wd1T, 512,
                                                         (size_t)1024 * 512);
   k_gemm_x6_bt<<<dim3(8, 16), 256, 0, stream>>>(XSp, (size_t)2048 * 512, Wd1T,
                                                 (size_t)1024 * 512, Xp1, 2048, 1024, 512);
   k_src_dst<<<2048, 256, 0, stream>>>(Xp1, asd1, add1, src1, dst1, 4, 256);
   k_transpose_split<<<dim3(4, 32, 4), 256, 0, stream>>>(Xp1, 1024, 256, XpS, 2048, PS1);
-  k_gat_x6<<<dim3(8, 16, 2), 512, 0, stream>>>(A1, 2048, XpS, PS1, src1, dst1, P, dPp, 1024,
-                                               256, 1024);
-  k_gat_reduce<<<2048, 256, 0, stream>>>(P, 2, (size_t)2048 * 1024, dPp, (size_t)2048 * 4, bd1,
-                                         X1, 1024, 256, 2048 * 1024);
+  k_gat_x6<<<dim3(8, 16, 4), 512, 0, stream>>>(A1, 2048, XpS, PS1, src1, dst1, P, dPp, 1024,
+                                               256, 2, 512);
+  k_gat_reduce<<<2048, 256, 0, stream>>>(P, 4, (size_t)2048 * 1024, dPp, (size_t)2048 * 4, bd1,
+                                         X1, nullptr, 1024, 256, 2048 * 1024);
   k_score<<<512, 256, 0, stream>>>(X1, wp1, bp1, sc1, 1024);
-  k_topk_rank<<<8, 256, 2048 * 8, stream>>>(sc1, 2048, 1024, idx1, v1);
+  k_topk_rank<<<8, 256, 2048 * 8, stream>>>(sc1, 2048, 1024, idx1, v1, nullptr);
   k_gather_mat<<<dim3(4, 1024), 256, 0, stream>>>(A1, 2048, idx1, A2m, 1024);
-  k_gather_scale_rows<<<dim3(4, 1024), 256, 0, stream>>>(X1, 1024, idx1, v1, X2in);
-
-  k_f32_to_bf16<<<1024, 256, 0, stream>>>(X2in, X2inB, 1024 * 1024);
+  k_gather_scale_b16<<<dim3(1, 1024), 256, 0, stream>>>(X1, 1024, idx1, v1, X2inB);
+
   k_transpose_bf16<<<dim3(16, 16), 256, 0, stream>>>(Wb, 1024, WbT, 1024, 1024);
   k_gemm_mfma_bt<<<dim3(8, 8), 256, 0, stream>>>(X2inB, WbT, nullptr, Xpb, 1024, 1024, 1024);
   k_src_dst<<<1024, 128, 0, stream>>>(Xpb, asb, adb, srcb, dstb, 2, 512);
   k_transpose_bf16h<<<dim3(8, 16, 2), 256, 0, stream>>>(Xpb, 1024, 512, XpT, 1024);
-  k_gat_mfma<<<dim3(16, 4, 8), 256, 0, stream>>>(A2m, 1024, XpT, srcb, dstb, P, dPp, 1024, 512,
-                                                 128);
-  k_gat_reduce<<<1024, 256, 0, stream>>>(P, 8, (size_t)1024 * 1024, dPp, (size_t)1024 * 2, bb,
-                                         Xb, 1024, 512, 1024 * 1024);
-
-  k_f32_to_bf16<<<1024, 256, 0, stream>>>(Xb, XbB, 1024 * 1024);
+  k_gat_b16<4, 1><<<dim3(2, 8, 4), 512, 0, stream>>>(A2m, 1024, XpT, srcb, dstb, P, dPp, 1024,
+                                                     512, 256);
+  k_gat_reduce<<<1024, 256, 0, stream>>>(P, 4, (size_t)1024 * 1024, dPp, (size_t)1024 * 2, bb,
+                                         nullptr, XbB, 1024, 512, 1024 * 1024);
+
   k_transpose_bf16<<<dim3(8, 16), 256, 0, stream>>>(Wu0, 512, Wu0T, 1024, 512);
   k_gemm_mfma_bt<<<dim3(4, 8), 256, 0, stream>>>(XbB, Wu0T, nullptr, Pu0, 1024, 512, 1024);
   k_fill0<<<1024, 256, 0, stream>>>(Xpu0, 2048 * 512);
   k_scatter_rows<<<dim3(2, 1024), 256, 0, stream>>>(Pu0, 512, idx1, Xpu0);
   k_src_dst<<<2048, 256, 0, stream>>>(Xpu0, asu0, adu0, su0, du0, 4, 128);
   k_transpose_bf16h<<<dim3(2, 32, 4), 256, 0, stream>>>(Xpu0, 512, 128, XpT, 2048);
-  k_gat_mfma<<<dim3(8, 8, 8), 256, 0, stream>>>(A1, 2048, XpT, su0, du0, P, dPp, 512, 128, 256);
+  k_gat_b16<4, 4><<<dim3(1, 16, 8), 512, 0, stream>>>(A1, 2048, XpT, su0, du0, P, dPp, 512,
+                                                      128, 256);
   k_gat_reduce<<<1024, 256, 0, stream>>>(P, 8, (size_t)2048 * 512, dPp, (size_t)2048 * 4, bu0,
-                                         Xu0, 512, 128, 2048 * 512);
-  k_f32_to_bf16<<<1024, 256, 0, stream>>>(Xu0, Xu0B, 2048 * 512);
+                                         nullptr, Xu0B, 512, 128, 2048 * 512);
 
   k_transpose_bf16<<<dim3(4, 8), 256, 0, stream>>>(Wu1, 256, Wu1T, 512, 256);
   k_gemm_mfma_bt<<<dim3(2, 16), 256, 0, stream>>>(Xu0B, Wu1T, nullptr, Pu1, 2048, 256, 512);
@@ -966,11 +955,11 @@
   k_scatter_rows<<<dim3(1, 2048), 256, 0, stream>>>(Pu1, 256, idx0, Xpu1);
   k_src_dst<<<4096, 256, 0, stream>>>(Xpu1, asu1, adu1, su1, du1, 4, 64);
   k_transpose_bf16h<<<dim3(1, 64, 4), 256, 0, stream>>>(Xpu1, 256, 64, XpT, 4096);
-  k_gat_mfma<<<dim3(4, 16, 8), 256, 0, stream>>>(A0, 4096, XpT, su1, du1, P, dPp, 256, 64, 512);
+  k_gat_b16<2, 4><<<dim3(1, 32, 8), 512, 0, stream>>>(A0, 4096, XpT, su1, du1, P, dPp, 256,
+                                                      64, 512);
   k_gat_reduce<<<1024, 256, 0, stream>>>(P, 8, (size_t)4096 * 256, dPp, (size_t)4096 * 4, bu1,
-                                         Xu1, 256, 64, 4096 * 256);
-  k_f32_to_bf16<<<1024, 256, 0, stream>>>(Xu1, Xu1B, 4096 * 256);
-  k_transpose_bf16<<<dim3(4, 64), 256, 0, stream>>>(Xu1, 256, Xu1T, 4096, 256);
+                                         nullptr, Xu1B, 256, 64, 4096 * 256);
+  k_transpose_bb<<<dim3(4, 64), 256, 0, stream>>>(Xu1B, 256, Xu1T, 4096, 256);
 
   k_gemm_aup<<<dim3(4, 64), 512, 0, stream>>>(Wup, Xu1T, Pz, 8192, 4096, 1024);
   k_softmax_fuse<<<8192, 256, 0, stream>>>(Pz, 4, (size_t)8192 * 256, bup, ZB);
```

After: 960.9 us, median of 2. -16.0%, faster.
